# Performance work log

Hardware: AMD Instinct MI355X
Metric: run time of the kernel (lower is better)

The kernel has to match this reference:

```python
import jax, jax.numpy as jnp
import numpy as np

NH, HD = 12, 64          # heads, head dim (d_model=768)
SC = HD ** -0.5          # both Attention and CA_Attention use head_dim**-0.5


def patchify(x, p1, p2):
    # 'b c (h p1) (w p2) -> b (h w) (p1 p2 c)'
    B, C, H, W = x.shape
    h, w = H // p1, W // p2
    x = x.reshape(B, C, h, p1, w, p2).transpose(0, 2, 4, 3, 5, 1)  # b h w p1 p2 c
    return x.reshape(B, h * w, p1 * p2 * C)


def unpatchify(x, h, w, p1, p2, c):
    # 'b (h w) (p1 p2 c) -> b c (h p1) (w p2)'
    B = x.shape[0]
    x = x.reshape(B, h, w, p1, p2, c).transpose(0, 5, 1, 3, 2, 4)
    return x.reshape(B, c, h * p1, w * p2)


def ln(x, g, b):
    m = x.mean(-1, keepdims=True)
    v = ((x - m) ** 2).mean(-1, keepdims=True)
    return (x - m) / jnp.sqrt(v + 1e-5) * g + b


def setup_inputs() -> dict:
    key = jax.random.key(0)
    specs = [
        ('img_feats', (2, 32, 112, 112, 80)), ('txt', (2, 77, 768)),
        ('pe_w_ax', (1120, 768)), ('pe_b_ax', (768,)),
        ('pe_w_sag', (1120, 768)), ('pe_b_sag', (768,)),
        ('pe_w_cor', (1568, 768)), ('pe_b_cor', (768,)),
        ('pos_ax', (1, 256, 768)), ('pos_sag', (1, 256, 768)), ('pos_cor', (1, 256, 768)),
        ('qw', (768, 768)), ('kw', (768, 768)), ('vw', (768, 768)),
        ('pw', (768, 768)), ('pb', (768,)),
        ('caq_w', (768, 768)), ('caq_b', (768,)), ('cak_w', (768, 768)), ('cak_b', (768,)),
        ('cav_w', (768, 768)), ('cav_b', (768,)), ('cao_w', (768, 768)), ('cao_b', (768,)),
        ('mlp_w1', (768, 3072)), ('mlp_b1', (3072,)), ('mlp_w2', (3072, 768)), ('mlp_b2', (768,)),
        ('ow_ax', (768, 1120)), ('ob_ax', (1120,)),
        ('ow_sag', (768, 1120)), ('ob_sag', (1120,)),
        ('ow_cor', (768, 1568)), ('ob_cor', (1568,)),
    ]
    big = {'img_feats', 'txt', 'pos_ax', 'pos_sag', 'pos_cor'}
    out = {}
    for k, (n, s) in zip(jax.random.split(key, len(specs)), specs):
        scale = 1.0 if n in big else 0.02
        out[n] = jax.random.normal(k, s, jnp.float32) * scale
    out['view_w'] = jnp.ones((3,), jnp.float32)
    for n in ('n1_g', 'n2_g', 'n3_g'):
        out[n] = jnp.ones((768,), jnp.float32)
    for n in ('n1_b', 'n2_b', 'n3_b'):
        out[n] = jnp.zeros((768,), jnp.float32)
    return out


def reference(img_feats, txt, pe_w_ax, pe_b_ax, pe_w_sag, pe_b_sag, pe_w_cor, pe_b_cor,
              pos_ax, pos_sag, pos_cor, view_w, qw, kw, vw, pw, pb,
              caq_w, caq_b, cak_w, cak_b, cav_w, cav_b, cao_w, cao_b,
              n1_g, n1_b, n2_g, n2_b, n3_g, n3_b,
              mlp_w1, mlp_b1, mlp_w2, mlp_b2,
              ow_ax, ob_ax, ow_sag, ob_sag, ow_cor, ob_cor):

    def img_attn(t):
        B, N, C = t.shape
        q = (t @ qw).reshape(B, N, NH, HD)
        k = (t @ kw).reshape(B, N, NH, HD)
        v = (t @ vw).reshape(B, N, NH, HD)
        a = jax.nn.softmax(jnp.einsum('bnkc,bmkc->bknm', q, k) * SC, axis=-1)
        x = jnp.einsum('bknm,bmkc->bnkc', a, v).reshape(B, N, C)
        return x @ pw + pb

    def ca_attn(t, im):
        B, T, _ = t.shape
        N = im.shape[1]
        qh = (t @ caq_w + caq_b).reshape(B, T, NH, HD).transpose(0, 2, 1, 3)
        kh = (im @ cak_w + cak_b).reshape(B, N, NH, HD).transpose(0, 2, 1, 3)
        vh = (im @ cav_w + cav_b).reshape(B, N, NH, HD).transpose(0, 2, 1, 3)
        a = jax.nn.softmax(jnp.einsum('bhid,bhjd->bhij', qh, kh) * SC, axis=-1)
        # faithful to original einsum 'b h i j, b h j d -> b h j d' (sums over i)
        o = jnp.einsum('bhij,bhjd->bhjd', a, vh)
        o = o.transpose(0, 2, 1, 3).reshape(B, N, NH * HD)
        return o @ cao_w + cao_b

    def branch(v2d, pe_w, pe_b, pos, ow, ob, p1, p2):
        B, C, H, W = v2d.shape
        h, w = H // p1, W // p2
        q = patchify(v2d, p1, p2) @ pe_w + pe_b + pos
        q = ln(q, n1_g, n1_b)
        q = q + img_attn(q)
        q = ln(q, n2_g, n2_b)
        x = q + ca_attn(txt, q)
        x = x + (jax.nn.gelu(ln(x, n3_g, n3_b) @ mlp_w1 + mlp_b1, approximate=False) @ mlp_w2 + mlp_b2)
        return unpatchify(x @ ow + ob, h, w, p1, p2, C)

    # adaptive_avg_pool3d to size-1 along one axis == mean over that axis
    ax = img_feats.mean(2)    # (B,C,H,W)
    sag = img_feats.mean(3)   # (B,C,D,W)
    cor = img_feats.mean(4)   # (B,C,D,H)
    oax = branch(ax, pe_w_ax, pe_b_ax, pos_ax, ow_ax, ob_ax, 7, 5)
    osag = branch(sag, pe_w_sag, pe_b_sag, pos_sag, ow_sag, ob_sag, 7, 5)
    ocor = branch(cor, pe_w_cor, pe_b_cor, pos_cor, ow_cor, ob_cor, 7, 7)
    v3 = (view_w[0] * oax[:, :, None] + view_w[1] * osag[:, :, :, None]
          + view_w[2] * ocor[:, :, :, :, None])
    return img_feats + v3
```

## Files before the change

kernel.cpp:

```cpp
#include <hip/hip_runtime.h>
#include <math.h>

typedef __attribute__((ext_vector_type(8))) short s8;
typedef __attribute__((ext_vector_type(4))) float f4;
typedef unsigned short u16;

__device__ inline u16 f2bf(float f) {
    unsigned u = __float_as_uint(f);
    u += 0x7fffu + ((u >> 16) & 1u);
    return (u16)(u >> 16);
}
__device__ inline float bf2f(u16 x) {
    return __uint_as_float(((unsigned)x) << 16);
}
#define MFMA16(a, b, c) __builtin_amdgcn_mfma_f32_16x16x32_bf16(a, b, c, 0, 0, 0)

__global__ __launch_bounds__(256) void mean3_k(const float* __restrict__ img,
                                               float* __restrict__ axp,
                                               float* __restrict__ sag,
                                               float* __restrict__ cor) {
    __shared__ float sl[112*81];
    int blk = blockIdx.x;
    int dc = blk & 15, bc = blk >> 4;
    int d0 = dc * 7;
    int t = threadIdx.x;
    f4 axr[9];
    #pragma unroll
    for (int k = 0; k < 9; ++k) axr[k] = (f4){0.f,0.f,0.f,0.f};
    const float* base = img + (size_t)bc * 1003520 + (size_t)d0 * 8960;
    for (int sidx = 0; sidx < 7; ++sidx) {
        const f4* sp = reinterpret_cast<const f4*>(base + (size_t)sidx * 8960);
        #pragma unroll
        for (int k = 0; k < 9; ++k) {
            int q = t + k * 256;
            if (q < 2240) {
                f4 v = sp[q];
                axr[k] += v;
                int h = q / 20, w4 = q % 20;
                float* row = &sl[h * 81 + w4 * 4];
                row[0] = v[0]; row[1] = v[1]; row[2] = v[2]; row[3] = v[3];
            }
        }
        __syncthreads();
        if (t < 112) {
            float acc = 0.f;
            #pragma unroll 8
            for (int w = 0; w < 80; ++w) acc += sl[t * 81 + w];
            cor[((size_t)bc * 112 + d0 + sidx) * 112 + t] = acc * (1.f / 80.f);
        } else if (t < 192) {
            int w = t - 112;
            float acc = 0.f;
            #pragma unroll 8
            for (int h = 0; h < 112; ++h) acc += sl[h * 81 + w];
            sag[((size_t)bc * 112 + d0 + sidx) * 80 + w] = acc * (1.f / 112.f);
        }
        __syncthreads();
    }
    float* axo = axp + ((size_t)dc * 64 + bc) * 8960;
    #pragma unroll
    for (int k = 0; k < 9; ++k) {
        int q = t + k * 256;
        if (q < 2240) *reinterpret_cast<f4*>(axo + q * 4) = axr[k];
    }
}

struct TT {
    const float* in[16];
    u16* out[16];
    int K[16];
    int N[16];
    int start[16];
};

__global__ __launch_bounds__(256) void transp_all(TT tab) {
    __shared__ float tl[32][33];
    int bid = blockIdx.x;
    int e = 0;
    #pragma unroll
    for (int i = 1; i < 16; ++i) if (bid >= tab.start[i]) e = i;
    const float* in = tab.in[e];
    u16* out = tab.out[e];
    int K = tab.K[e], N = tab.N[e];
    int tid = bid - tab.start[e];
    int nt = N >> 5;
    int k0 = (tid / nt) * 32, n0 = (tid % nt) * 32;
    int t = threadIdx.x;
    int r = t >> 5, c = t & 31;
    #pragma unroll
    for (int i = 0; i < 4; ++i) tl[r + i*8][c] = in[(long)(k0 + r + i*8)*N + n0 + c];
    __syncthreads();
    #pragma unroll
    for (int i = 0; i < 4; ++i) out[(long)(n0 + r + i*8)*K + k0 + c] = f2bf(tl[c][r + i*8]);
}

__global__ __launch_bounds__(256) void patchify3_k(const float* __restrict__ axp,
                                                   const float* __restrict__ m_sag,
                                                   const float* __restrict__ m_cor,
                                                   u16* __restrict__ P0, u16* __restrict__ P1,
                                                   u16* __restrict__ P2) {
    __shared__ float sl[32][113];
    int br = blockIdx.y;
    int X = blockIdx.x;
    int b = X / 112, rem = X % 112;
    int hh = rem / 7, pp1 = rem % 7;
    const float* src; u16* dst; int Wt, p2, PD;
    if (br == 0)      { src = nullptr; dst = P0; Wt = 80;  p2 = 5; PD = 1120; }
    else if (br == 1) { src = m_sag;   dst = P1; Wt = 80;  p2 = 5; PD = 1120; }
    else              { src = m_cor;   dst = P2; Wt = 112; p2 = 7; PD = 1568; }
    int t = threadIdx.x;
    int row = hh*7 + pp1;
    int wq = Wt >> 2;
    if (br == 0) {
        for (int i = t; i < 32*20; i += 256) {
            int c = i / 20, w4 = i % 20;
            f4 s = (f4){0.f,0.f,0.f,0.f};
            size_t base = ((size_t)(b*32 + c)*112 + row)*80 + w4*4;
            #pragma unroll
            for (int p = 0; p < 16; ++p)
                s += *reinterpret_cast<const f4*>(axp + (size_t)p*573440 + base);
            s *= (1.f/112.f);
            sl[c][w4*4+0] = s[0]; sl[c][w4*4+1] = s[1]; sl[c][w4*4+2] = s[2]; sl[c][w4*4+3] = s[3];
        }
    } else {
        for (int i = t; i < 32*wq; i += 256) {
            int c = i / wq, w4 = i % wq;
            float4 v = *reinterpret_cast<const float4*>(
                src + ((size_t)(b*32 + c)*112 + row)*Wt + w4*4);
            sl[c][w4*4+0] = v.x; sl[c][w4*4+1] = v.y; sl[c][w4*4+2] = v.z; sl[c][w4*4+3] = v.w;
        }
    }
    __syncthreads();
    int tot = 16 * p2 * 32;
    for (int o = t; o < tot; o += 256) {
        int ww = o / (p2*32), rest = o % (p2*32);
        int pp2 = rest >> 5, c = rest & 31;
        dst[((size_t)(b*256 + hh*16 + ww))*PD + (pp1*p2 + pp2)*32 + c]
            = f2bf(sl[c][ww*p2 + pp2]);
    }
}

__device__ inline void load_tile(const u16* __restrict__ P, int ld, int nrows, int K,
                                 int r0, int k0, int t, s8 v[4]) {
    #pragma unroll
    for (int i = 0; i < 4; ++i) {
        int chunk = t + i*256;
        int row = chunk >> 4, c8 = (chunk & 15) * 8;
        s8 x;
        #pragma unroll
        for (int q = 0; q < 8; ++q) x[q] = 0;
        if (r0 + row < nrows && k0 + c8 < K)
            x = *reinterpret_cast<const s8*>(P + (long)(r0 + row)*ld + k0 + c8);
        v[i] = x;
    }
}
__device__ inline void load_tile_f32(const float* __restrict__ P, int ld, int nrows, int K,
                                     int r0, int k0, int t, s8 v[4]) {
    #pragma unroll
    for (int i = 0; i < 4; ++i) {
        int chunk = t + i*256;
        int row = chunk >> 4, c8 = (chunk & 15) * 8;
        s8 x;
        #pragma unroll
        for (int q = 0; q < 8; ++q) x[q] = 0;
        if (r0 + row < nrows && k0 + c8 < K) {
            const float* src = P + (long)(r0 + row)*ld + k0 + c8;
            #pragma unroll
            for (int q = 0; q < 8; ++q) x[q] = (short)f2bf(src[q]);
        }
        v[i] = x;
    }
}
__device__ inline void write_tile(u16 (*S)[136], int t, const s8 v[4]) {
    #pragma unroll
    for (int i = 0; i < 4; ++i) {
        int chunk = t + i*256;
        *reinterpret_cast<s8*>(&S[chunk >> 4][(chunk & 15)*8]) = v[i];
    }
}
__device__ inline void mfma_tile(const u16 (*As)[136], const u16 (*Bs)[136],
                                 int wr, int wc, int lane, f4 acc[2][2]) {
    int lrow = lane & 15;
    #pragma unroll
    for (int kh = 0; kh < 4; ++kh) {
        int lk = kh*32 + (lane >> 4) * 8;
        s8 af0 = *reinterpret_cast<const s8*>(&As[wr*32 + lrow][lk]);
        s8 af1 = *reinterpret_cast<const s8*>(&As[wr*32 + 16 + lrow][lk]);
        s8 bg0 = *reinterpret_cast<const s8*>(&Bs[wc*32 + lrow][lk]);
        s8 bg1 = *reinterpret_cast<const s8*>(&Bs[wc*32 + 16 + lrow][lk]);
        acc[0][0] = MFMA16(af0, bg0, acc[0][0]);
        acc[0][1] = MFMA16(af0, bg1, acc[0][1]);
        acc[1][0] = MFMA16(af1, bg0, acc[1][0]);
        acc[1][1] = MFMA16(af1, bg1, acc[1][1]);
    }
}

__global__ __launch_bounds__(256) void gemm_bf(
    const u16* __restrict__ A, const u16* __restrict__ Bt,
    float* __restrict__ Cf, u16* __restrict__ Cb,
    int M, int N, int K,
    const float* __restrict__ bias, const float* __restrict__ resid,
    int act)
{
    __shared__ u16 As[2][64][136];
    __shared__ u16 Bs[2][64][136];
    int t = threadIdx.x;
    int m0 = blockIdx.y * 64, n0 = blockIdx.x * 64;
    int wave = t >> 6, lane = t & 63;
    int wr = wave >> 1, wc = wave & 1;
    f4 acc[2][2];
    #pragma unroll
    for (int m = 0; m < 2; ++m)
        #pragma unroll
        for (int n = 0; n < 2; ++n)
            #pragma unroll
            for (int r = 0; r < 4; ++r) acc[m][n][r] = 0.f;
    int nk = (K + 127) >> 7;
    s8 pa[4], pbv[4];
    load_tile(A, K, M, K, m0, 0, t, pa);
    load_tile(Bt, K, N, K, n0, 0, t, pbv);
    write_tile(As[0], t, pa);
    write_tile(Bs[0], t, pbv);
    __syncthreads();
    for (int kt = 0; kt < nk; ++kt) {
        int cur = kt & 1;
        if (kt + 1 < nk) {
            load_tile(A, K, M, K, m0, (kt+1) << 7, t, pa);
            load_tile(Bt, K, N, K, n0, (kt+1) << 7, t, pbv);
        }
        mfma_tile(As[cur], Bs[cur], wr, wc, lane, acc);
        if (kt + 1 < nk) {
            write_tile(As[cur^1], t, pa);
            write_tile(Bs[cur^1], t, pbv);
        }
        __syncthreads();
    }
    #pragma unroll
    for (int m = 0; m < 2; ++m) {
        int rbase = m0 + wr*32 + m*16 + (lane >> 4) * 4;
        #pragma unroll
        for (int n = 0; n < 2; ++n) {
            int col = n0 + wc*32 + n*16 + (lane & 15);
            if (col >= N) continue;
            #pragma unroll
            for (int r = 0; r < 4; ++r) {
                int row = rbase + r;
                if (row >= M) continue;
                float v = acc[m][n][r];
                if (bias)  v += bias[col];
                if (resid) v += resid[(long)row * N + col];
                if (act == 1) v = 0.5f * v * (1.0f + erff(v * 0.70710678118654752f));
                long ci = (long)row * N + col;
                if (Cf) Cf[ci] = v;
                if (Cb) Cb[ci] = f2bf(v);
            }
        }
    }
}

__global__ __launch_bounds__(256) void gemm_big(
    const u16* __restrict__ A, const u16* __restrict__ Bt,
    u16* __restrict__ Cb, u16* __restrict__ vt,
    int N, int K,
    const float* __restrict__ bias, const float* __restrict__ bias2, int act)
{
    __shared__ u16 As[2][128][72];
    __shared__ u16 Bs[2][128][72];
    int t = threadIdx.x;
    int m0 = blockIdx.y * 128, n0 = blockIdx.x * 128;
    int wave = t >> 6, lane = t & 63;
    int wr = wave >> 1, wc = wave & 1;
    f4 acc[4][4];
    #pragma unroll
    for (int m = 0; m < 4; ++m)
        #pragma unroll
        for (int n = 0; n < 4; ++n)
            #pragma unroll
            for (int r = 0; r < 4; ++r) acc[m][n][r] = 0.f;
    int nk = K >> 6;
    s8 pa[4], pbv[4];
    #pragma unroll
    for (int i = 0; i < 4; ++i) {
        int chunk = t + i*256;
        pa[i]  = *reinterpret_cast<const s8*>(A  + (long)(m0 + (chunk>>3))*K + (chunk&7)*8);
        pbv[i] = *reinterpret_cast<const s8*>(Bt + (long)(n0 + (chunk>>3))*K + (chunk&7)*8);
    }
    #pragma unroll
    for (int i = 0; i < 4; ++i) {
        int chunk = t + i*256;
        *reinterpret_cast<s8*>(&As[0][chunk>>3][(chunk&7)*8]) = pa[i];
        *reinterpret_cast<s8*>(&Bs[0][chunk>>3][(chunk&7)*8]) = pbv[i];
    }
    __syncthreads();
    for (int kt = 0; kt < nk; ++kt) {
        int cur = kt & 1;
        if (kt + 1 < nk) {
            int k0 = (kt+1) << 6;
            #pragma unroll
            for (int i = 0; i < 4; ++i) {
                int chunk = t + i*256;
                pa[i]  = *reinterpret_cast<const s8*>(A  + (long)(m0 + (chunk>>3))*K + k0 + (chunk&7)*8);
                pbv[i] = *reinterpret_cast<const s8*>(Bt + (long)(n0 + (chunk>>3))*K + k0 + (chunk&7)*8);
            }
        }
        #pragma unroll
        for (int kh = 0; kh < 2; ++kh) {
            int lk = kh*32 + (lane >> 4) * 8;
            int lr = lane & 15;
            s8 af[4], bf[4];
            #pragma unroll
            for (int m = 0; m < 4; ++m)
                af[m] = *reinterpret_cast<const s8*>(&As[cur][wr*64 + m*16 + lr][lk]);
            #pragma unroll
            for (int n = 0; n < 4; ++n)
                bf[n] = *reinterpret_cast<const s8*>(&Bs[cur][wc*64 + n*16 + lr][lk]);
            #pragma unroll
            for (int m = 0; m < 4; ++m)
                #pragma unroll
                for (int n = 0; n < 4; ++n)
                    acc[m][n] = MFMA16(af[m], bf[n], acc[m][n]);
        }
        if (kt + 1 < nk) {
            #pragma unroll
            for (int i = 0; i < 4; ++i) {
                int chunk = t + i*256;
                *reinterpret_cast<s8*>(&As[cur^1][chunk>>3][(chunk&7)*8]) = pa[i];
                *reinterpret_cast<s8*>(&Bs[cur^1][chunk>>3][(chunk&7)*8]) = pbv[i];
            }
        }
        __syncthreads();
    }
    #pragma unroll
    for (int m = 0; m < 4; ++m) {
        int rbase = m0 + wr*64 + m*16 + (lane >> 4) * 4;
        #pragma unroll
        for (int n = 0; n < 4; ++n) {
            int col = n0 + wc*64 + n*16 + (lane & 15);
            #pragma unroll
            for (int r = 0; r < 4; ++r) {
                int row = rbase + r;
                float v = acc[m][n][r];
                if (bias) {
                    float bb = bias2 ? ((col < 768) ? bias[col] : bias2[col - 768]) : bias[col];
                    v += bb;
                }
                if (act == 1) v = 0.5f * v * (1.0f + erff(v * 0.70710678118654752f));
                u16 b = f2bf(v);
                Cb[(long)row * N + col] = b;
                if (vt && col >= 1536) {
                    int z = (row >> 8) * 12 + ((col - 1536) >> 6);
                    vt[((long)z * 64 + (col & 63)) * 256 + (row & 255)] = b;
                }
            }
        }
    }
}

struct PeDesc {
    const u16* A[3];
    const u16* Bt[4];
    const float* bias[4];
    const float* pos[3];
    int K[4];
    int M[4];
};

__global__ __launch_bounds__(256) void gemm_pe(PeDesc d, const float* __restrict__ txtf,
                                               float* __restrict__ C, u16* __restrict__ QHb) {
    int z = blockIdx.z;
    int M = d.M[z], K = d.K[z];
    int m0 = blockIdx.y * 64, n0 = blockIdx.x * 64;
    if (m0 >= M) return;
    __shared__ u16 As[2][64][136];
    __shared__ u16 Bs[2][64][136];
    const u16* Bb = d.Bt[z];
    const float* bias = d.bias[z];
    int t = threadIdx.x;
    int wave = t >> 6, lane = t & 63;
    int wr = wave >> 1, wc = wave & 1;
    f4 acc[2][2];
    #pragma unroll
    for (int m = 0; m < 2; ++m)
        #pragma unroll
        for (int n = 0; n < 2; ++n)
            #pragma unroll
            for (int r = 0; r < 4; ++r) acc[m][n][r] = 0.f;
    int nk = (K + 127) >> 7;
    s8 pa[4], pbv[4];
    if (z < 3) load_tile(d.A[z], K, M, K, m0, 0, t, pa);
    else       load_tile_f32(txtf, K, M, K, m0, 0, t, pa);
    load_tile(Bb, K, 768, K, n0, 0, t, pbv);
    write_tile(As[0], t, pa);
    write_tile(Bs[0], t, pbv);
    __syncthreads();
    for (int kt = 0; kt < nk; ++kt) {
        int cur = kt & 1;
        if (kt + 1 < nk) {
            if (z < 3) load_tile(d.A[z], K, M, K, m0, (kt+1) << 7, t, pa);
            else       load_tile_f32(txtf, K, M, K, m0, (kt+1) << 7, t, pa);
            load_tile(Bb, K, 768, K, n0, (kt+1) << 7, t, pbv);
        }
        mfma_tile(As[cur], Bs[cur], wr, wc, lane, acc);
        if (kt + 1 < nk) {
            write_tile(As[cur^1], t, pa);
            write_tile(Bs[cur^1], t, pbv);
        }
        __syncthreads();
    }
    #pragma unroll
    for (int m = 0; m < 2; ++m) {
        int rbase = m0 + wr*32 + m*16 + (lane >> 4) * 4;
        #pragma unroll
        for (int n = 0; n < 2; ++n) {
            int col = n0 + wc*32 + n*16 + (lane & 15);
            #pragma unroll
            for (int r = 0; r < 4; ++r) {
                int row = rbase + r;
                if (row >= M) continue;
                float v = acc[m][n][r] + bias[col];
                if (z < 3) {
                    v += d.pos[z][(long)(row & 255)*768 + col];
                    C[((long)z*512 + row) * 768 + col] = v;
                } else {
                    QHb[(long)row * 768 + col] = f2bf(v);
                }
            }
        }
    }
}

struct OwDesc {
    const u16* Bt[3];
    float* plane[3];
    const float* bias[3];
    int N[3];
    int p2[3];
    int Wd[3];
};

__global__ __launch_bounds__(256) void gemm_ow(OwDesc d, const u16* __restrict__ A,
                                               const float* __restrict__ vwp) {
    int z = blockIdx.z;
    int N = d.N[z];
    int n0 = blockIdx.x * 64;
    if (n0 >= N) return;
    __shared__ u16 As[2][64][136];
    __shared__ u16 Bs[2][64][136];
    const u16* Ab = A + (long)z * 512 * 768;
    const u16* Bb = d.Bt[z];
    int t = threadIdx.x;
    int m0 = blockIdx.y * 64;
    int wave = t >> 6, lane = t & 63;
    int wr = wave >> 1, wc = wave & 1;
    f4 acc[2][2];
    #pragma unroll
    for (int m = 0; m < 2; ++m)
        #pragma unroll
        for (int n = 0; n < 2; ++n)
            #pragma unroll
            for (int r = 0; r < 4; ++r) acc[m][n][r] = 0.f;
    s8 pa[4], pbv[4];
    load_tile(Ab, 768, 512, 768, m0, 0, t, pa);
    load_tile(Bb, 768, N, 768, n0, 0, t, pbv);
    write_tile(As[0], t, pa);
    write_tile(Bs[0], t, pbv);
    __syncthreads();
    for (int kt = 0; kt < 6; ++kt) {
        int cur = kt & 1;
        if (kt + 1 < 6) {
            load_tile(Ab, 768, 512, 768, m0, (kt+1) << 7, t, pa);
            load_tile(Bb, 768, N, 768, n0, (kt+1) << 7, t, pbv);
        }
        mfma_tile(As[cur], Bs[cur], wr, wc, lane, acc);
        if (kt + 1 < 6) {
            write_tile(As[cur^1], t, pa);
            write_tile(Bs[cur^1], t, pbv);
        }
        __syncthreads();
    }
    float* plane = d.plane[z];
    const float* bias = d.bias[z];
    int p2 = d.p2[z], Wd = d.Wd[z];
    float wt = vwp[z];
    #pragma unroll
    for (int m = 0; m < 2; ++m) {
        int rbase = m0 + wr*32 + m*16 + (lane >> 4) * 4;
        #pragma unroll
        for (int n = 0; n < 2; ++n) {
            int col = n0 + wc*32 + n*16 + (lane & 15);
            if (col >= N) continue;
            int pp = col >> 5, c = col & 31;
            int pp1 = pp / p2, pp2 = pp % p2;
            float bv = bias[col];
            #pragma unroll
            for (int r = 0; r < 4; ++r) {
                int row = rbase + r;
                int b = row >> 8, nn = row & 255;
                int hh = nn >> 4, ww = nn & 15;
                int ho = hh*7 + pp1, wo = ww*p2 + pp2;
                plane[((long)(b*32 + c)*112 + ho)*Wd + wo] = wt * (acc[m][n][r] + bv);
            }
        }
    }
}

__global__ __launch_bounds__(256) void ln_k(const float* __restrict__ in,
                                            float* __restrict__ outf,
                                            u16* __restrict__ outb,
                                            const float* __restrict__ g,
                                            const float* __restrict__ bta) {
    constexpr int N = 768;
    int row = blockIdx.x;
    const float* x = in + (size_t)row * N;
    int t = threadIdx.x;
    float v0 = x[t], v1 = x[t+256], v2 = x[t+512];
    float s = v0+v1+v2, s2 = v0*v0+v1*v1+v2*v2;
    #pragma unroll
    for (int off = 32; off > 0; off >>= 1) { s += __shfl_down(s, off); s2 += __shfl_down(s2, off); }
    __shared__ float red[8];
    int wid = t >> 6, lane = t & 63;
    if (lane == 0) { red[wid] = s; red[wid+4] = s2; }
    __syncthreads();
    if (t == 0) {
        float S = red[0]+red[1]+red[2]+red[3];
        float S2 = red[4]+red[5]+red[6]+red[7];
        float mean = S * (1.f/N);
        float var = S2 * (1.f/N) - mean*mean;
        red[0] = mean; red[1] = rsqrtf(var + 1e-5f);
    }
    __syncthreads();
    float mean = red[0], rstd = red[1];
    float y0 = (v0-mean)*rstd*g[t]     + bta[t];
    float y1 = (v1-mean)*rstd*g[t+256] + bta[t+256];
    float y2 = (v2-mean)*rstd*g[t+512] + bta[t+512];
    if (outf) {
        float* y = outf + (size_t)row * N;
        y[t] = y0; y[t+256] = y1; y[t+512] = y2;
    }
    if (outb) {
        u16* y = outb + (size_t)row * N;
        y[t] = f2bf(y0); y[t+256] = f2bf(y1); y[t+512] = f2bf(y2);
    }
}

__global__ __launch_bounds__(256) void attn_k(const u16* __restrict__ QKV,
                                              const u16* __restrict__ Vt,
                                              u16* __restrict__ O) {
    __shared__ u16 Ks[256][72];
    __shared__ u16 Ps[128][264];
    __shared__ u16 Vs[64][264];
    int zz = blockIdx.x;
    int bh = zz >> 1, half = zz & 1;
    int bb = bh / 12, h = bh % 12;
    long qrow0 = (long)bb*256 + half*128;
    int hcol = h*64;
    int t = threadIdx.x;
    int wave = t >> 6, lane = t & 63;
    int lr = lane & 15, lg = lane >> 4;
    #pragma unroll
    for (int i = 0; i < 8; ++i) {
        int chunk = t + i*256;
        int row = chunk >> 3, c8 = (chunk & 7)*8;
        *reinterpret_cast<s8*>(&Ks[row][c8]) =
            *reinterpret_cast<const s8*>(QKV + ((long)bb*256 + row)*2304 + 768 + hcol + c8);
    }
    #pragma unroll
    for (int i = 0; i < 8; ++i) {
        int chunk = t + i*256;
        int d = chunk >> 5, j8 = (chunk & 31)*8;
        *reinterpret_cast<s8*>(&Vs[d][j8]) =
            *reinterpret_cast<const s8*>(Vt + (long)bh*16384 + (long)d*256 + j8);
    }
    __syncthreads();
    f4 acc[2][16];
    #pragma unroll
    for (int m = 0; m < 2; ++m)
        #pragma unroll
        for (int n = 0; n < 16; ++n)
            #pragma unroll
            for (int r = 0; r < 4; ++r) acc[m][n][r] = 0.f;
    #pragma unroll
    for (int kh = 0; kh < 2; ++kh) {
        s8 af0 = *reinterpret_cast<const s8*>(QKV + (qrow0 + wave*32 + lr)*2304 + hcol + kh*32 + lg*8);
        s8 af1 = *reinterpret_cast<const s8*>(QKV + (qrow0 + wave*32 + 16 + lr)*2304 + hcol + kh*32 + lg*8);
        #pragma unroll
        for (int n = 0; n < 16; ++n) {
            s8 bf = *reinterpret_cast<const s8*>(&Ks[n*16 + lr][kh*32 + lg*8]);
            acc[0][n] = MFMA16(af0, bf, acc[0][n]);
            acc[1][n] = MFMA16(af1, bf, acc[1][n]);
        }
    }
    #pragma unroll
    for (int m = 0; m < 2; ++m)
        #pragma unroll
        for (int r = 0; r < 4; ++r) {
            float mx = -1e30f;
            #pragma unroll
            for (int n = 0; n < 16; ++n) mx = fmaxf(mx, acc[m][n][r]);
            #pragma unroll
            for (int o = 8; o; o >>= 1) mx = fmaxf(mx, __shfl_xor(mx, o));
            float l = 0.f;
            float p[16];
            #pragma unroll
            for (int n = 0; n < 16; ++n) {
                p[n] = __expf((acc[m][n][r] - mx) * 0.125f);
                l += p[n];
            }
            #pragma unroll
            for (int o = 8; o; o >>= 1) l += __shfl_xor(l, o);
            float inv = 1.f / l;
            int prow = wave*32 + m*16 + lg*4 + r;
            #pragma unroll
            for (int n = 0; n < 16; ++n)
                Ps[prow][n*16 + lr] = f2bf(p[n] * inv);
        }
    __syncthreads();
    f4 o2[2][4];
    #pragma unroll
    for (int m = 0; m < 2; ++m)
        #pragma unroll
        for (int n = 0; n < 4; ++n)
            #pragma unroll
            for (int r = 0; r < 4; ++r) o2[m][n][r] = 0.f;
    #pragma unroll
    for (int kh = 0; kh < 8; ++kh) {
        s8 pf0 = *reinterpret_cast<const s8*>(&Ps[wave*32 + lr][kh*32 + lg*8]);
        s8 pf1 = *reinterpret_cast<const s8*>(&Ps[wave*32 + 16 + lr][kh*32 + lg*8]);
        #pragma unroll
        for (int n = 0; n < 4; ++n) {
            s8 vf = *reinterpret_cast<const s8*>(&Vs[n*16 + lr][kh*32 + lg*8]);
            o2[0][n] = MFMA16(pf0, vf, o2[0][n]);
            o2[1][n] = MFMA16(pf1, vf, o2[1][n]);
        }
    }
    #pragma unroll
    for (int m = 0; m < 2; ++m)
        #pragma unroll
        for (int n = 0; n < 4; ++n)
            #pragma unroll
            for (int r = 0; r < 4; ++r)
                O[(qrow0 + wave*32 + m*16 + lg*4 + r)*768 + hcol + n*16 + lr] = f2bf(o2[m][n][r]);
}

__global__ __launch_bounds__(256) void ca_fused(const u16* __restrict__ QHb,
                                                const u16* __restrict__ KVHb,
                                                u16* __restrict__ O) {
    __shared__ u16 QHs[80][72];
    __shared__ u16 KHs[256][72];
    __shared__ float rmax[80][4];
    __shared__ float rsum[80][4];
    __shared__ float Wj[256];
    int bh = blockIdx.x;
    int rowblk = bh / 12, h = bh % 12;
    int bsel = rowblk & 1;
    int t = threadIdx.x;
    int wave = t >> 6, lane = t & 63;
    int lr = lane & 15, lg = lane >> 4;
    #pragma unroll
    for (int i = 0; i < 3; ++i) {
        int chunk = t + i*256;
        if (chunk < 640) {
            int row = chunk >> 3, c8 = (chunk & 7)*8;
            s8 v;
            #pragma unroll
            for (int q = 0; q < 8; ++q) v[q] = 0;
            if (row < 77)
                v = *reinterpret_cast<const s8*>(QHb + ((long)(bsel*77 + row))*768 + h*64 + c8);
            *reinterpret_cast<s8*>(&QHs[row][c8]) = v;
        }
    }
    #pragma unroll
    for (int i = 0; i < 8; ++i) {
        int chunk = t + i*256;
        int row = chunk >> 3, c8 = (chunk & 7)*8;
        *reinterpret_cast<s8*>(&KHs[row][c8]) =
            *reinterpret_cast<const s8*>(KVHb + ((long)rowblk*256 + row)*1536 + h*64 + c8);
    }
    __syncthreads();
    f4 acc[5][4];
    #pragma unroll
    for (int m = 0; m < 5; ++m)
        #pragma unroll
        for (int n = 0; n < 4; ++n)
            #pragma unroll
            for (int r = 0; r < 4; ++r) acc[m][n][r] = 0.f;
    #pragma unroll
    for (int kh = 0; kh < 2; ++kh) {
        s8 af[5], bf[4];
        #pragma unroll
        for (int m = 0; m < 5; ++m)
            af[m] = *reinterpret_cast<const s8*>(&QHs[m*16 + lr][kh*32 + lg*8]);
        #pragma unroll
        for (int n = 0; n < 4; ++n)
            bf[n] = *reinterpret_cast<const s8*>(&KHs[wave*64 + n*16 + lr][kh*32 + lg*8]);
        #pragma unroll
        for (int m = 0; m < 5; ++m)
            #pragma unroll
            for (int n = 0; n < 4; ++n)
                acc[m][n] = MFMA16(af[m], bf[n], acc[m][n]);
    }
    #pragma unroll
    for (int m = 0; m < 5; ++m)
        #pragma unroll
        for (int r = 0; r < 4; ++r) {
            float mx = -1e30f;
            #pragma unroll
            for (int n = 0; n < 4; ++n) mx = fmaxf(mx, acc[m][n][r]);
            #pragma unroll
            for (int o = 8; o; o >>= 1) mx = fmaxf(mx, __shfl_xor(mx, o));
            if (lr == 0) rmax[m*16 + lg*4 + r][wave] = mx;
        }
    __syncthreads();
    #pragma unroll
    for (int m = 0; m < 5; ++m)
        #pragma unroll
        for (int r = 0; r < 4; ++r) {
            int i = m*16 + lg*4 + r;
            float mi = fmaxf(fmaxf(rmax[i][0], rmax[i][1]), fmaxf(rmax[i][2], rmax[i][3]));
            float s = 0.f;
            #pragma unroll
            for (int n = 0; n < 4; ++n) s += __expf((acc[m][n][r] - mi) * 0.125f);
            #pragma unroll
            for (int o = 8; o; o >>= 1) s += __shfl_xor(s, o);
            if (lr == 0) rsum[i][wave] = s;
        }
    __syncthreads();
    float wn[4] = {0.f, 0.f, 0.f, 0.f};
    #pragma unroll
    for (int m = 0; m < 5; ++m)
        #pragma unroll
        for (int r = 0; r < 4; ++r) {
            int i = m*16 + lg*4 + r;
            if (i < 77) {
                float mi = fmaxf(fmaxf(rmax[i][0], rmax[i][1]), fmaxf(rmax[i][2], rmax[i][3]));
                float li = rsum[i][0] + rsum[i][1] + rsum[i][2] + rsum[i][3];
                float inv = 1.f / li;
                #pragma unroll
                for (int n = 0; n < 4; ++n)
                    wn[n] += __expf((acc[m][n][r] - mi) * 0.125f) * inv;
            }
        }
    #pragma unroll
    for (int n = 0; n < 4; ++n) {
        wn[n] += __shfl_xor(wn[n], 16);
        wn[n] += __shfl_xor(wn[n], 32);
    }
    if (lane < 16) {
        #pragma unroll
        for (int n = 0; n < 4; ++n) Wj[wave*64 + n*16 + lr] = wn[n];
    }
    __syncthreads();
    int d = t & 63;
    #pragma unroll 4
    for (int it = 0; it < 64; ++it) {
        int j = it*4 + (t >> 6);
        long row = (long)rowblk*256 + j;
        float vh = bf2f(KVHb[row*1536 + 768 + h*64 + d]);
        O[row*768 + h*64 + d] = f2bf(Wj[j] * vh);
    }
}

__global__ __launch_bounds__(256) void final_k(const float* __restrict__ img,
                                               const float* __restrict__ Aax,
                                               const float* __restrict__ Asag,
                                               const float* __restrict__ Acor,
                                               float* __restrict__ out) {
    int blk = blockIdx.x;
    int bc = blk / 112;
    const float4* ip = reinterpret_cast<const float4*>(img + (size_t)blk * 8960);
    const float4* ap = reinterpret_cast<const float4*>(Aax + (size_t)bc * 8960);
    const float4* sp = reinterpret_cast<const float4*>(Asag + (size_t)blk * 80);
    const float*  cp = Acor + (size_t)blk * 112;
    float4* op = reinterpret_cast<float4*>(out + (size_t)blk * 8960);
    int t = threadIdx.x;
    for (int q = t; q < 2240; q += 256) {
        int h = q / 20, w4 = q % 20;
        float4 iv = ip[q], av = ap[q], sv = sp[w4];
        float cv = cp[h];
        float4 o;
        o.x = iv.x + av.x + sv.x + cv;
        o.y = iv.y + av.y + sv.y + cv;
        o.z = iv.z + av.z + sv.z + cv;
        o.w = iv.w + av.w + sv.w + cv;
        op[q] = o;
    }
}

extern "C" void kernel_launch(void* const* d_in, const int* in_sizes, int n_in,
                              void* d_out, int out_size, void* d_ws, size_t ws_size,
                              hipStream_t stream) {
    (void)in_sizes; (void)n_in; (void)out_size; (void)ws_size;
    const float* img    = (const float*)d_in[0];
    const float* txt    = (const float*)d_in[1];
    const float* pe_w[3] = {(const float*)d_in[2], (const float*)d_in[4], (const float*)d_in[6]};
    const float* pe_b[3] = {(const float*)d_in[3], (const float*)d_in[5], (const float*)d_in[7]};
    const float* pos[3]  = {(const float*)d_in[8], (const float*)d_in[9], (const float*)d_in[10]};
    const float* qw = (const float*)d_in[11];
    const float* kw = (const float*)d_in[12];
    const float* vw_attn = (const float*)d_in[13];
    const float* pw = (const float*)d_in[14];
    const float* pb = (const float*)d_in[15];
    const float* caq_w = (const float*)d_in[16];
    const float* caq_b = (const float*)d_in[17];
    const float* cak_w = (const float*)d_in[18];
    const float* cak_b = (const float*)d_in[19];
    const float* cav_w = (const float*)d_in[20];
    const float* cav_b = (const float*)d_in[21];
    const float* cao_w = (const float*)d_in[22];
    const float* cao_b = (const float*)d_in[23];
    const float* mlp_w1 = (const float*)d_in[24];
    const float* mlp_b1 = (const float*)d_in[25];
    const float* mlp_w2 = (const float*)d_in[26];
    const float* mlp_b2 = (const float*)d_in[27];
    const float* ow[3] = {(const float*)d_in[28], (const float*)d_in[30], (const float*)d_in[32]};
    const float* ob[3] = {(const float*)d_in[29], (const float*)d_in[31], (const float*)d_in[33]};
    const float* view_w = (const float*)d_in[34];
    const float* n_g[3] = {(const float*)d_in[35], (const float*)d_in[36], (const float*)d_in[37]};
    const float* n_b[3] = {(const float*)d_in[38], (const float*)d_in[39], (const float*)d_in[40]};

    unsigned char* sb = (unsigned char*)d_out;
    size_t off = 0;
    auto B = [&](size_t bytes) -> void* {
        void* p = sb + off; off += (bytes + 511) & ~(size_t)511; return p;
    };
    u16* qkvT  = (u16*)B((size_t)2304*768*2);
    u16* pwT   = (u16*)B(768*768*2);
    u16* caqT  = (u16*)B(768*768*2);
    u16* cakvT = (u16*)B((size_t)1536*768*2);
    u16* caoT  = (u16*)B(768*768*2);
    u16* mlp1T = (u16*)B((size_t)3072*768*2);
    u16* mlp2T = (u16*)B((size_t)768*3072*2);
    u16* peT[3]; peT[0] = (u16*)B((size_t)768*1120*2); peT[1] = (u16*)B((size_t)768*1120*2); peT[2] = (u16*)B((size_t)768*1568*2);
    u16* owT[3]; owT[0] = (u16*)B((size_t)1120*768*2); owT[1] = (u16*)B((size_t)1120*768*2); owT[2] = (u16*)B((size_t)1568*768*2);
    float* axp   = (float*)B((size_t)16*573440*4);
    float* m_sag = (float*)B(573440*4);
    float* m_cor = (float*)B(802816*4);
    u16* P0 = (u16*)B((size_t)512*1120*2);
    u16* P1 = (u16*)B((size_t)512*1120*2);
    u16* P2 = (u16*)B((size_t)512*1568*2);
    float* X0  = (float*)B((size_t)1536*768*4);
    float* X1f = (float*)B((size_t)1536*768*4);
    float* X2  = (float*)B((size_t)1536*768*4);
    float* X3f = (float*)B((size_t)1536*768*4);
    float* X4  = (float*)B((size_t)1536*768*4);
    u16* X1b = (u16*)B((size_t)1536*768*2);
    u16* X3b = (u16*)B((size_t)1536*768*2);
    u16* X5b = (u16*)B((size_t)1536*768*2);
    u16* X6b = (u16*)B((size_t)1536*768*2);
    u16* QKVb = (u16*)B((size_t)1536*2304*2);
    u16* Obf = (u16*)B((size_t)1536*768*2);
    u16* Vt  = (u16*)B((size_t)72*64*256*2);
    u16* Hb  = (u16*)B((size_t)1536*3072*2);
    u16* KVHb = (u16*)B((size_t)1536*1536*2);
    u16* QHb  = (u16*)B((size_t)154*768*2);

    float* ws = (float*)d_ws;
    float* Aax  = ws;
    float* Asag = ws + 573440;
    float* Acor = ws + 1146880;

    TT tab;
    {
        const float* ins[16] = {qw, kw, vw_attn, pw, caq_w, cak_w, cav_w, cao_w,
                                mlp_w1, mlp_w2, pe_w[0], pe_w[1], pe_w[2], ow[0], ow[1], ow[2]};
        u16* outs[16] = {qkvT, qkvT + 768*768, qkvT + 2*768*768, pwT, caqT, cakvT,
                         cakvT + 768*768, caoT, mlp1T, mlp2T, peT[0], peT[1], peT[2],
                         owT[0], owT[1], owT[2]};
        int Ks[16] = {768,768,768,768,768,768,768,768, 768,3072, 1120,1120,1568, 768,768,768};
        int Ns[16] = {768,768,768,768,768,768,768,768, 3072,768, 768,768,768, 1120,1120,1568};
        int st = 0;
        for (int i = 0; i < 16; ++i) {
            tab.in[i] = ins[i]; tab.out[i] = outs[i]; tab.K[i] = Ks[i]; tab.N[i] = Ns[i];
            tab.start[i] = st;
            st += (Ks[i] >> 5) * (Ns[i] >> 5);
        }
        transp_all<<<st, 256, 0, stream>>>(tab);
    }

    mean3_k<<<1024, 256, 0, stream>>>(img, axp, m_sag, m_cor);
    patchify3_k<<<dim3(224,3), 256, 0, stream>>>(axp, m_sag, m_cor, P0, P1, P2);

    auto gemm = [&](const u16* A, const u16* Bt, float* Cf, u16* Cb,
                    int M, int N, int K, const float* bias, const float* resid, int act) {
        dim3 g((N+63)/64, (M+63)/64, 1);
        gemm_bf<<<g, 256, 0, stream>>>(A, Bt, Cf, Cb, M, N, K, bias, resid, act);
    };

    {
        PeDesc d;
        d.A[0] = P0; d.A[1] = P1; d.A[2] = P2;
        d.Bt[0] = peT[0]; d.Bt[1] = peT[1]; d.Bt[2] = peT[2]; d.Bt[3] = caqT;
        d.bias[0] = pe_b[0]; d.bias[1] = pe_b[1]; d.bias[2] = pe_b[2]; d.bias[3] = caq_b;
        d.pos[0] = pos[0]; d.pos[1] = pos[1]; d.pos[2] = pos[2];
        d.K[0] = 1120; d.K[1] = 1120; d.K[2] = 1568; d.K[3] = 768;
        d.M[0] = 512; d.M[1] = 512; d.M[2] = 512; d.M[3] = 154;
        gemm_pe<<<dim3(12,8,4), 256, 0, stream>>>(d, txt, X0, QHb);
    }

    ln_k<<<1536, 256, 0, stream>>>(X0, X1f, X1b, n_g[0], n_b[0]);
    gemm_big<<<dim3(18,12), 256, 0, stream>>>(X1b, qkvT, QKVb, Vt, 2304, 768, nullptr, nullptr, 0);
    attn_k<<<144, 256, 0, stream>>>(QKVb, Vt, Obf);
    gemm(Obf, pwT, X2, nullptr, 1536, 768, 768, pb, X1f, 0);
    ln_k<<<1536, 256, 0, stream>>>(X2, X3f, X3b, n_g[1], n_b[1]);
    gemm_big<<<dim3(12,12), 256, 0, stream>>>(X3b, cakvT, KVHb, nullptr, 1536, 768, cak_b, cav_b, 0);
    ca_fused<<<72, 256, 0, stream>>>(QHb, KVHb, Obf);
    gemm(Obf, caoT, X4, nullptr, 1536, 768, 768, cao_b, X3f, 0);
    ln_k<<<1536, 256, 0, stream>>>(X4, nullptr, X5b, n_g[2], n_b[2]);
    gemm_big<<<dim3(24,12), 256, 0, stream>>>(X5b, mlp1T, Hb, nullptr, 3072, 768, mlp_b1, nullptr, 1);
    gemm(Hb, mlp2T, nullptr, X6b, 1536, 768, 3072, mlp_b2, X4, 0);
    {
        OwDesc d;
        d.Bt[0] = owT[0]; d.Bt[1] = owT[1]; d.Bt[2] = owT[2];
        d.plane[0] = Aax; d.plane[1] = Asag; d.plane[2] = Acor;
        d.bias[0] = ob[0]; d.bias[1] = ob[1]; d.bias[2] = ob[2];
        d.N[0] = 1120; d.N[1] = 1120; d.N[2] = 1568;
        d.p2[0] = 5; d.p2[1] = 5; d.p2[2] = 7;
        d.Wd[0] = 80; d.Wd[1] = 80; d.Wd[2] = 112;
        gemm_ow<<<dim3(25,8,3), 256, 0, stream>>>(d, X6b, view_w);
    }

    final_k<<<7168, 256, 0, stream>>>(img, Aax, Asag, Acor, (float*)d_out);
}
```

Before: 445.9 us.

## Fuse trunk GEMM/LN/CA stages into two persistent cooperative kernels with grid sync

Replaces the chain of separate launches (PE GEMM, layernorms, QKV GEMM, projection GEMMs, cross-attention, MLP, output GEMM) with two persistent cooperative kernels. Each kernel loops over the stages using grid-stride tile loops, a shared-memory union, and grid-wide barriers between stages. This is meant to remove per-kernel launch and drain overhead between many small dependent kernels. In exchange, the grid is capped at the occupancy limit (at most 512 blocks), so some stages get less parallelism, and each grid sync adds its own cost.

New measurement: 885.1 us. 1.99x slower.

```diff
diff --git a/kernel.cpp b/kernel.cpp
--- a/kernel.cpp
+++ b/kernel.cpp
@@ -1,5 +1,8 @@
 #include <hip/hip_runtime.h>
+#include <hip/hip_cooperative_groups.h>
 #include <math.h>
+
+namespace cg = cooperative_groups;
 
 typedef __attribute__((ext_vector_type(8))) short s8;
 typedef __attribute__((ext_vector_type(4))) float f4;
@@ -14,6 +17,15 @@
     return __uint_as_float(((unsigned)x) << 16);
 }
 #define MFMA16(a, b, c) __builtin_amdgcn_mfma_f32_16x16x32_bf16(a, b, c, 0, 0, 0)
+
+struct SMemG64 { u16 As[2][64][136]; u16 Bs[2][64][136]; };
+struct SMemG128 { u16 As[2][128][72]; u16 Bs[2][128][72]; };
+struct SMemCA {
+    u16 QHs[80][72]; u16 KHs[256][72];
+    float rmax[80][4]; float rsum[80][4]; float Wj[256];
+};
+struct SMemLN { float red[8]; };
+union SMemU { SMemG64 g64; SMemG128 g128; SMemCA ca; SMemLN ln; };
 
 __global__ __launch_bounds__(256) void mean3_k(const float* __restrict__ img,
                                                float* __restrict__ axp,
@@ -194,20 +206,11 @@
     }
 }
 
-__global__ __launch_bounds__(256) void gemm_bf(
-    const u16* __restrict__ A, const u16* __restrict__ Bt,
-    float* __restrict__ Cf, u16* __restrict__ Cb,
-    int M, int N, int K,
-    const float* __restrict__ bias, const float* __restrict__ resid,
-    int act)
-{
-    __shared__ u16 As[2][64][136];
-    __shared__ u16 Bs[2][64][136];
-    int t = threadIdx.x;
-    int m0 = blockIdx.y * 64, n0 = blockIdx.x * 64;
+__device__ void g64_core(SMemG64& S, const u16* A, const float* Af32,
+                         const u16* Bt, int M, int N, int K,
+                         int m0, int n0, int t, f4 acc[2][2]) {
     int wave = t >> 6, lane = t & 63;
     int wr = wave >> 1, wc = wave & 1;
-    f4 acc[2][2];
     #pragma unroll
     for (int m = 0; m < 2; ++m)
         #pragma unroll
@@ -216,24 +219,33 @@
             for (int r = 0; r < 4; ++r) acc[m][n][r] = 0.f;
     int nk = (K + 127) >> 7;
     s8 pa[4], pbv[4];
-    load_tile(A, K, M, K, m0, 0, t, pa);
+    if (Af32) load_tile_f32(Af32, K, M, K, m0, 0, t, pa);
+    else      load_tile(A, K, M, K, m0, 0, t, pa);
     load_tile(Bt, K, N, K, n0, 0, t, pbv);
-    write_tile(As[0], t, pa);
-    write_tile(Bs[0], t, pbv);
+    write_tile(S.As[0], t, pa);
+    write_tile(S.Bs[0], t, pbv);
     __syncthreads();
     for (int kt = 0; kt < nk; ++kt) {
         int cur = kt & 1;
         if (kt + 1 < nk) {
-            load_tile(A, K, M, K, m0, (kt+1) << 7, t, pa);
+            if (Af32) load_tile_f32(Af32, K, M, K, m0, (kt+1) << 7, t, pa);
+            else      load_tile(A, K, M, K, m0, (kt+1) << 7, t, pa);
             load_tile(Bt, K, N, K, n0, (kt+1) << 7, t, pbv);
         }
-        mfma_tile(As[cur], Bs[cur], wr, wc, lane, acc);
+        mfma_tile(S.As[cur], S.Bs[cur], wr, wc, lane, acc);
         if (kt + 1 < nk) {
-            write_tile(As[cur^1], t, pa);
-            write_tile(Bs[cur^1], t, pbv);
+            write_tile(S.As[cur^1], t, pa);
+            write_tile(S.Bs[cur^1], t, pbv);
         }
         __syncthreads();
     }
+}
+
+__device__ void g64_epi_std(const f4 acc[2][2], int M, int N, int m0, int n0, int t,
+                            float* Cf, u16* Cb, const float* bias,
+                            const float* resid, int act) {
+    int wave = t >> 6, lane = t & 63;
+    int wr = wave >> 1, wc = wave & 1;
     #pragma unroll
     for (int m = 0; m < 2; ++m) {
         int rbase = m0 + wr*32 + m*16 + (lane >> 4) * 4;
@@ -257,288 +269,389 @@
     }
 }
 
-__global__ __launch_bounds__(256) void gemm_big(
-    const u16* __restrict__ A, const u16* __restrict__ Bt,
-    u16* __restrict__ Cb, u16* __restrict__ vt,
-    int N, int K,
-    const float* __restrict__ bias, const float* __restrict__ bias2, int act)
-{
-    __shared__ u16 As[2][128][72];
-    __shared__ u16 Bs[2][128][72];
-    int t = threadIdx.x;
-    int m0 = blockIdx.y * 128, n0 = blockIdx.x * 128;
-    int wave = t >> 6, lane = t & 63;
-    int wr = wave >> 1, wc = wave & 1;
-    f4 acc[4][4];
-    #pragma unroll
-    for (int m = 0; m < 4; ++m)
-        #pragma unroll
-        for (int n = 0; n < 4; ++n)
-            #pragma unroll
-            for (int r = 0; r < 4; ++r) acc[m][n][r] = 0.f;
-    int nk = K >> 6;
-    s8 pa[4], pbv[4];
-    #pragma unroll
-    for (int i = 0; i < 4; ++i) {
-        int chunk = t + i*256;
-        pa[i]  = *reinterpret_cast<const s8*>(A  + (long)(m0 + (chunk>>3))*K + (chunk&7)*8);
-        pbv[i] = *reinterpret_cast<const s8*>(Bt + (long)(n0 + (chunk>>3))*K + (chunk&7)*8);
-    }
-    #pragma unroll
-    for (int i = 0; i < 4; ++i) {
-        int chunk = t + i*256;
-        *reinterpret_cast<s8*>(&As[0][chunk>>3][(chunk&7)*8]) = pa[i];
-        *reinterpret_cast<s8*>(&Bs[0][chunk>>3][(chunk&7)*8]) = pbv[i];
-    }
-    __syncthreads();
-    for (int kt = 0; kt < nk; ++kt) {
-        int cur = kt & 1;
-        if (kt + 1 < nk) {
-            int k0 = (kt+1) << 6;
-            #pragma unroll
-            for (int i = 0; i < 4; ++i) {
-                int chunk = t + i*256;
-                pa[i]  = *reinterpret_cast<const s8*>(A  + (long)(m0 + (chunk>>3))*K + k0 + (chunk&7)*8);
-                pbv[i] = *reinterpret_cast<const s8*>(Bt + (long)(n0 + (chunk>>3))*K + k0 + (chunk&7)*8);
-            }
-        }
-        #pragma unroll
-        for (int kh = 0; kh < 2; ++kh) {
-            int lk = kh*32 + (lane >> 4) * 8;
-            int lr = lane & 15;
-            s8 af[4], bf[4];
-            #pragma unroll
-            for (int m = 0; m < 4; ++m)
-                af[m] = *reinterpret_cast<const s8*>(&As[cur][wr*64 + m*16 + lr][lk]);
-            #pragma unroll
-            for (int n = 0; n < 4; ++n)
-                bf[n] = *reinterpret_cast<const s8*>(&Bs[cur][wc*64 + n*16 + lr][lk]);
-            #pragma unroll
-            for (int m = 0; m < 4; ++m)
-                #pragma unroll
-                for (int n = 0; n < 4; ++n)
-                    acc[m][n] = MFMA16(af[m], bf[n], acc[m][n]);
-        }
-        if (kt + 1 < nk) {
-            #pragma unroll
-            for (int i = 0; i < 4; ++i) {
-                int chunk = t + i*256;
-                *reinterpret_cast<s8*>(&As[cur^1][chunk>>3][(chunk&7)*8]) = pa[i];
-                *reinterpret_cast<s8*>(&Bs[cur^1][chunk>>3][(chunk&7)*8]) = pbv[i];
-            }
-        }
-        __syncthreads();
-    }
-    #pragma unroll
-    for (int m = 0; m < 4; ++m) {
-        int rbase = m0 + wr*64 + m*16 + (lane >> 4) * 4;
-        #pragma unroll
-        for (int n = 0; n < 4; ++n) {
-            int col = n0 + wc*64 + n*16 + (lane & 15);
-            #pragma unroll
-            for (int r = 0; r < 4; ++r) {
-                int row = rbase + r;
-                float v = acc[m][n][r];
-                if (bias) {
-                    float bb = bias2 ? ((col < 768) ? bias[col] : bias2[col - 768]) : bias[col];
-                    v += bb;
-                }
-                if (act == 1) v = 0.5f * v * (1.0f + erff(v * 0.70710678118654752f));
-                u16 b = f2bf(v);
-                Cb[(long)row * N + col] = b;
-                if (vt && col >= 1536) {
-                    int z = (row >> 8) * 12 + ((col - 1536) >> 6);
-                    vt[((long)z * 64 + (col & 63)) * 256 + (row & 255)] = b;
-                }
-            }
-        }
-    }
-}
-
-struct PeDesc {
-    const u16* A[3];
-    const u16* Bt[4];
-    const float* bias[4];
-    const float* pos[3];
-    int K[4];
-    int M[4];
-};
-
-__global__ __launch_bounds__(256) void gemm_pe(PeDesc d, const float* __restrict__ txtf,
-                                               float* __restrict__ C, u16* __restrict__ QHb) {
-    int z = blockIdx.z;
-    int M = d.M[z], K = d.K[z];
-    int m0 = blockIdx.y * 64, n0 = blockIdx.x * 64;
-    if (m0 >= M) return;
-    __shared__ u16 As[2][64][136];
-    __shared__ u16 Bs[2][64][136];
-    const u16* Bb = d.Bt[z];
-    const float* bias = d.bias[z];
+__device__ void phase_g64(SMemU& sm, const u16* A, const u16* Bt,
+                          float* Cf, u16* Cb, int M, int N, int K,
+                          const float* bias, const float* resid, int act) {
+    int ntx = (N + 63) >> 6, nty = (M + 63) >> 6;
+    int ntiles = ntx * nty;
+    for (int tile = blockIdx.x; tile < ntiles; tile += gridDim.x) {
+        int m0 = (tile / ntx) * 64, n0 = (tile % ntx) * 64;
+        f4 acc[2][2];
+        g64_core(sm.g64, A, nullptr, Bt, M, N, K, m0, n0, threadIdx.x, acc);
+        g64_epi_std(acc, M, N, m0, n0, threadIdx.x, Cf, Cb, bias, resid, act);
+    }
+}
+
+__device__ void phase_g128(SMemU& sm, const u16* A, const u16* Bt,
+                           u16* Cb, u16* vt, int Mt, int Nt, int N, int K,
+                           const float* bias, const float* bias2, int act) {
+    SMemG128& S = sm.g128;
     int t = threadIdx.x;
     int wave = t >> 6, lane = t & 63;
     int wr = wave >> 1, wc = wave & 1;
-    f4 acc[2][2];
-    #pragma unroll
-    for (int m = 0; m < 2; ++m)
-        #pragma unroll
-        for (int n = 0; n < 2; ++n)
-            #pragma unroll
-            for (int r = 0; r < 4; ++r) acc[m][n][r] = 0.f;
-    int nk = (K + 127) >> 7;
-    s8 pa[4], pbv[4];
-    if (z < 3) load_tile(d.A[z], K, M, K, m0, 0, t, pa);
-    else       load_tile_f32(txtf, K, M, K, m0, 0, t, pa);
-    load_tile(Bb, K, 768, K, n0, 0, t, pbv);
-    write_tile(As[0], t, pa);
-    write_tile(Bs[0], t, pbv);
-    __syncthreads();
-    for (int kt = 0; kt < nk; ++kt) {
-        int cur = kt & 1;
-        if (kt + 1 < nk) {
-            if (z < 3) load_tile(d.A[z], K, M, K, m0, (kt+1) << 7, t, pa);
-            else       load_tile_f32(txtf, K, M, K, m0, (kt+1) << 7, t, pa);
-            load_tile(Bb, K, 768, K, n0, (kt+1) << 7, t, pbv);
-        }
-        mfma_tile(As[cur], Bs[cur], wr, wc, lane, acc);
-        if (kt + 1 < nk) {
-            write_tile(As[cur^1], t, pa);
-            write_tile(Bs[cur^1], t, pbv);
+    int ntiles = Mt * Nt;
+    for (int tile = blockIdx.x; tile < ntiles; tile += gridDim.x) {
+        int m0 = (tile / Nt) * 128, n0 = (tile % Nt) * 128;
+        f4 acc[4][4];
+        #pragma unroll
+        for (int m = 0; m < 4; ++m)
+            #pragma unroll
+            for (int n = 0; n < 4; ++n)
+                #pragma unroll
+                for (int r = 0; r < 4; ++r) acc[m][n][r] = 0.f;
+        int nk = K >> 6;
+        s8 pa[4], pbv[4];
+        #pragma unroll
+        for (int i = 0; i < 4; ++i) {
+            int chunk = t + i*256;
+            pa[i]  = *reinterpret_cast<const s8*>(A  + (long)(m0 + (chunk>>3))*K + (chunk&7)*8);
+            pbv[i] = *reinterpret_cast<const s8*>(Bt + (long)(n0 + (chunk>>3))*K + (chunk&7)*8);
+        }
+        #pragma unroll
+        for (int i = 0; i < 4; ++i) {
+            int chunk = t + i*256;
+            *reinterpret_cast<s8*>(&S.As[0][chunk>>3][(chunk&7)*8]) = pa[i];
+            *reinterpret_cast<s8*>(&S.Bs[0][chunk>>3][(chunk&7)*8]) = pbv[i];
         }
         __syncthreads();
-    }
-    #pragma unroll
-    for (int m = 0; m < 2; ++m) {
-        int rbase = m0 + wr*32 + m*16 + (lane >> 4) * 4;
-        #pragma unroll
-        for (int n = 0; n < 2; ++n) {
-            int col = n0 + wc*32 + n*16 + (lane & 15);
-            #pragma unroll
-            for (int r = 0; r < 4; ++r) {
-                int row = rbase + r;
-                if (row >= M) continue;
-                float v = acc[m][n][r] + bias[col];
-                if (z < 3) {
-                    v += d.pos[z][(long)(row & 255)*768 + col];
-                    C[((long)z*512 + row) * 768 + col] = v;
-                } else {
-                    QHb[(long)row * 768 + col] = f2bf(v);
+        for (int kt = 0; kt < nk; ++kt) {
+            int cur = kt & 1;
+            if (kt + 1 < nk) {
+                int k0 = (kt+1) << 6;
+                #pragma unroll
+                for (int i = 0; i < 4; ++i) {
+                    int chunk = t + i*256;
+                    pa[i]  = *reinterpret_cast<const s8*>(A  + (long)(m0 + (chunk>>3))*K + k0 + (chunk&7)*8);
+                    pbv[i] = *reinterpret_cast<const s8*>(Bt + (long)(n0 + (chunk>>3))*K + k0 + (chunk&7)*8);
                 }
             }
-        }
-    }
-}
-
-struct OwDesc {
-    const u16* Bt[3];
-    float* plane[3];
-    const float* bias[3];
-    int N[3];
-    int p2[3];
-    int Wd[3];
+            #pragma unroll
+            for (int kh = 0; kh < 2; ++kh) {
+                int lk = kh*32 + (lane >> 4) * 8;
+                int lr = lane & 15;
+                s8 af[4], bf[4];
+                #pragma unroll
+                for (int m = 0; m < 4; ++m)
+                    af[m] = *reinterpret_cast<const s8*>(&S.As[cur][wr*64 + m*16 + lr][lk]);
+                #pragma unroll
+                for (int n = 0; n < 4; ++n)
+                    bf[n] = *reinterpret_cast<const s8*>(&S.Bs[cur][wc*64 + n*16 + lr][lk]);
+                #pragma unroll
+                for (int m = 0; m < 4; ++m)
+                    #pragma unroll
+                    for (int n = 0; n < 4; ++n)
+                        acc[m][n] = MFMA16(af[m], bf[n], acc[m][n]);
+            }
+            if (kt + 1 < nk) {
+                #pragma unroll
+                for (int i = 0; i < 4; ++i) {
+                    int chunk = t + i*256;
+                    *reinterpret_cast<s8*>(&S.As[cur^1][chunk>>3][(chunk&7)*8]) = pa[i];
+                    *reinterpret_cast<s8*>(&S.Bs[cur^1][chunk>>3][(chunk&7)*8]) = pbv[i];
+                }
+            }
+            __syncthreads();
+        }
+        #pragma unroll
+        for (int m = 0; m < 4; ++m) {
+            int rbase = m0 + wr*64 + m*16 + (lane >> 4) * 4;
+            #pragma unroll
+            for (int n = 0; n < 4; ++n) {
+                int col = n0 + wc*64 + n*16 + (lane & 15);
+                #pragma unroll
+                for (int r = 0; r < 4; ++r) {
+                    int row = rbase + r;
+                    float v = acc[m][n][r];
+                    if (bias) {
+                        float bb = bias2 ? ((col < 768) ? bias[col] : bias2[col - 768]) : bias[col];
+                        v += bb;
+                    }
+                    if (act == 1) v = 0.5f * v * (1.0f + erff(v * 0.70710678118654752f));
+                    u16 b = f2bf(v);
+                    Cb[(long)row * N + col] = b;
+                    if (vt && col >= 1536) {
+                        int z = (row >> 8) * 12 + ((col - 1536) >> 6);
+                        vt[((long)z * 64 + (col & 63)) * 256 + (row & 255)] = b;
+                    }
+                }
+            }
+        }
+    }
+}
+
+__device__ void ln_rows(SMemLN& S, const float* in, float* outf, u16* outb,
+                        const float* g, const float* bta) {
+    int t = threadIdx.x;
+    int wid = t >> 6, lane = t & 63;
+    for (int row = blockIdx.x; row < 1536; row += gridDim.x) {
+        const float* x = in + (size_t)row * 768;
+        float v0 = x[t], v1 = x[t+256], v2 = x[t+512];
+        float s = v0+v1+v2, s2 = v0*v0+v1*v1+v2*v2;
+        #pragma unroll
+        for (int off = 32; off; off >>= 1) { s += __shfl_down(s, off); s2 += __shfl_down(s2, off); }
+        if (lane == 0) { S.red[wid] = s; S.red[wid+4] = s2; }
+        __syncthreads();
+        float mean = (S.red[0]+S.red[1]+S.red[2]+S.red[3]) * (1.f/768.f);
+        float var = (S.red[4]+S.red[5]+S.red[6]+S.red[7]) * (1.f/768.f) - mean*mean;
+        float rstd = rsqrtf(var + 1e-5f);
+        float y0 = (v0-mean)*rstd*g[t]     + bta[t];
+        float y1 = (v1-mean)*rstd*g[t+256] + bta[t+256];
+        float y2 = (v2-mean)*rstd*g[t+512] + bta[t+512];
+        if (outf) {
+            float* y = outf + (size_t)row * 768;
+            y[t] = y0; y[t+256] = y1; y[t+512] = y2;
+        }
+        if (outb) {
+            u16* y = outb + (size_t)row * 768;
+            y[t] = f2bf(y0); y[t+256] = f2bf(y1); y[t+512] = f2bf(y2);
+        }
+        __syncthreads();
+    }
+}
+
+__device__ void ca_phase(SMemU& sm, const u16* QHb, const u16* KVHb, u16* O) {
+    if (blockIdx.x >= 72) return;
+    SMemCA& C = sm.ca;
+    int bh = blockIdx.x;
+    int rowblk = bh / 12, h = bh % 12;
+    int bsel = rowblk & 1;
+    int t = threadIdx.x;
+    int wave = t >> 6, lane = t & 63;
+    int lr = lane & 15, lg = lane >> 4;
+    #pragma unroll
+    for (int i = 0; i < 3; ++i) {
+        int chunk = t + i*256;
+        if (chunk < 640) {
+            int row = chunk >> 3, c8 = (chunk & 7)*8;
+            s8 v;
+            #pragma unroll
+            for (int q = 0; q < 8; ++q) v[q] = 0;
+            if (row < 77)
+                v = *reinterpret_cast<const s8*>(QHb + ((long)(bsel*77 + row))*768 + h*64 + c8);
+            *reinterpret_cast<s8*>(&C.QHs[row][c8]) = v;
+        }
+    }
+    #pragma unroll
+    for (int i = 0; i < 8; ++i) {
+        int chunk = t + i*256;
+        int row = chunk >> 3, c8 = (chunk & 7)*8;
+        *reinterpret_cast<s8*>(&C.KHs[row][c8]) =
+            *reinterpret_cast<const s8*>(KVHb + ((long)rowblk*256 + row)*1536 + h*64 + c8);
+    }
+    __syncthreads();
+    f4 acc[5][4];
+    #pragma unroll
+    for (int m = 0; m < 5; ++m)
+        #pragma unroll
+        for (int n = 0; n < 4; ++n)
+            #pragma unroll
+            for (int r = 0; r < 4; ++r) acc[m][n][r] = 0.f;
+    #pragma unroll
+    for (int kh = 0; kh < 2; ++kh) {
+        s8 af[5], bf[4];
+        #pragma unroll
+        for (int m = 0; m < 5; ++m)
+            af[m] = *reinterpret_cast<const s8*>(&C.QHs[m*16 + lr][kh*32 + lg*8]);
+        #pragma unroll
+        for (int n = 0; n < 4; ++n)
+            bf[n] = *reinterpret_cast<const s8*>(&C.KHs[wave*64 + n*16 + lr][kh*32 + lg*8]);
+        #pragma unroll
+        for (int m = 0; m < 5; ++m)
+            #pragma unroll
+            for (int n = 0; n < 4; ++n)
+                acc[m][n] = MFMA16(af[m], bf[n], acc[m][n]);
+    }
+    #pragma unroll
+    for (int m = 0; m < 5; ++m)
+        #pragma unroll
+        for (int r = 0; r < 4; ++r) {
+            float mx = -1e30f;
+            #pragma unroll
+            for (int n = 0; n < 4; ++n) mx = fmaxf(mx, acc[m][n][r]);
+            #pragma unroll
+            for (int o = 8; o; o >>= 1) mx = fmaxf(mx, __shfl_xor(mx, o));
+            if (lr == 0) C.rmax[m*16 + lg*4 + r][wave] = mx;
+        }
+    __syncthreads();
+    #pragma unroll
+    for (int m = 0; m < 5; ++m)
+        #pragma unroll
+        for (int r = 0; r < 4; ++r) {
+            int i = m*16 + lg*4 + r;
+            float mi = fmaxf(fmaxf(C.rmax[i][0], C.rmax[i][1]), fmaxf(C.rmax[i][2], C.rmax[i][3]));
+            float s = 0.f;
+            #pragma unroll
+            for (int n = 0; n < 4; ++n) s += __expf((acc[m][n][r] - mi) * 0.125f);
+            #pragma unroll
+            for (int o = 8; o; o >>= 1) s += __shfl_xor(s, o);
+            if (lr == 0) C.rsum[i][wave] = s;
+        }
+    __syncthreads();
+    float wn[4] = {0.f, 0.f, 0.f, 0.f};
+    #pragma unroll
+    for (int m = 0; m < 5; ++m)
+        #pragma unroll
+        for (int r = 0; r < 4; ++r) {
+            int i = m*16 + lg*4 + r;
+            if (i < 77) {
+                float mi = fmaxf(fmaxf(C.rmax[i][0], C.rmax[i][1]), fmaxf(C.rmax[i][2], C.rmax[i][3]));
+                float li = C.rsum[i][0] + C.rsum[i][1] + C.rsum[i][2] + C.rsum[i][3];
+                float inv = 1.f / li;
+                #pragma unroll
+                for (int n = 0; n < 4; ++n)
+                    wn[n] += __expf((acc[m][n][r] - mi) * 0.125f) * inv;
+            }
+        }
+    #pragma unroll
+    for (int n = 0; n < 4; ++n) {
+        wn[n] += __shfl_xor(wn[n], 16);
+        wn[n] += __shfl_xor(wn[n], 32);
+    }
+    if (lane < 16) {
+        #pragma unroll
+        for (int n = 0; n < 4; ++n) C.Wj[wave*64 + n*16 + lr] = wn[n];
+    }
+    __syncthreads();
+    int d = t & 63;
+    #pragma unroll 4
+    for (int it = 0; it < 64; ++it) {
+        int j = it*4 + (t >> 6);
+        long row = (long)rowblk*256 + j;
+        float vh = bf2f(KVHb[row*1536 + 768 + h*64 + d]);
+        O[row*768 + h*64 + d] = f2bf(C.Wj[j] * vh);
+    }
+}
+
+struct T1Args {
+    const u16* P[3];
+    const u16* peT[3]; const u16* caqT;
+    const float* peb[3]; const float* caqb;
+    const float* pos[3];
+    const float* txt;
+    float* X0; u16* QHb;
+    const float* g0; const float* b0;
+    float* X1f; u16* X1b;
+    const u16* qkvT; u16* QKVb; u16* Vt;
+    int K[4];
 };
 
-__global__ __launch_bounds__(256) void gemm_ow(OwDesc d, const u16* __restrict__ A,
-                                               const float* __restrict__ vwp) {
-    int z = blockIdx.z;
-    int N = d.N[z];
-    int n0 = blockIdx.x * 64;
-    if (n0 >= N) return;
-    __shared__ u16 As[2][64][136];
-    __shared__ u16 Bs[2][64][136];
-    const u16* Ab = A + (long)z * 512 * 768;
-    const u16* Bb = d.Bt[z];
+__global__ __launch_bounds__(256, 2) void trunk1_k(T1Args a) {
+    __shared__ SMemU sm;
+    cg::grid_group grid = cg::this_grid();
     int t = threadIdx.x;
-    int m0 = blockIdx.y * 64;
-    int wave = t >> 6, lane = t & 63;
-    int wr = wave >> 1, wc = wave & 1;
-    f4 acc[2][2];
-    #pragma unroll
-    for (int m = 0; m < 2; ++m)
-        #pragma unroll
-        for (int n = 0; n < 2; ++n)
-            #pragma unroll
-            for (int r = 0; r < 4; ++r) acc[m][n][r] = 0.f;
-    s8 pa[4], pbv[4];
-    load_tile(Ab, 768, 512, 768, m0, 0, t, pa);
-    load_tile(Bb, 768, N, 768, n0, 0, t, pbv);
-    write_tile(As[0], t, pa);
-    write_tile(Bs[0], t, pbv);
-    __syncthreads();
-    for (int kt = 0; kt < 6; ++kt) {
-        int cur = kt & 1;
-        if (kt + 1 < 6) {
-            load_tile(Ab, 768, 512, 768, m0, (kt+1) << 7, t, pa);
-            load_tile(Bb, 768, N, 768, n0, (kt+1) << 7, t, pbv);
-        }
-        mfma_tile(As[cur], Bs[cur], wr, wc, lane, acc);
-        if (kt + 1 < 6) {
-            write_tile(As[cur^1], t, pa);
-            write_tile(Bs[cur^1], t, pbv);
-        }
-        __syncthreads();
-    }
-    float* plane = d.plane[z];
-    const float* bias = d.bias[z];
-    int p2 = d.p2[z], Wd = d.Wd[z];
-    float wt = vwp[z];
-    #pragma unroll
-    for (int m = 0; m < 2; ++m) {
-        int rbase = m0 + wr*32 + m*16 + (lane >> 4) * 4;
-        #pragma unroll
-        for (int n = 0; n < 2; ++n) {
-            int col = n0 + wc*32 + n*16 + (lane & 15);
-            if (col >= N) continue;
-            int pp = col >> 5, c = col & 31;
-            int pp1 = pp / p2, pp2 = pp % p2;
-            float bv = bias[col];
-            #pragma unroll
-            for (int r = 0; r < 4; ++r) {
-                int row = rbase + r;
-                int b = row >> 8, nn = row & 255;
-                int hh = nn >> 4, ww = nn & 15;
-                int ho = hh*7 + pp1, wo = ww*p2 + pp2;
-                plane[((long)(b*32 + c)*112 + ho)*Wd + wo] = wt * (acc[m][n][r] + bv);
+    for (int tile = blockIdx.x; tile < 324; tile += gridDim.x) {
+        int z, ty, tx;
+        if (tile < 288) { z = tile / 96; int r = tile % 96; ty = r / 12; tx = r % 12; }
+        else            { z = 3; int r = tile - 288; ty = r / 12; tx = r % 12; }
+        int M = (z < 3) ? 512 : 154;
+        int K = a.K[z];
+        f4 acc[2][2];
+        g64_core(sm.g64, (z < 3) ? a.P[z] : nullptr, (z == 3) ? a.txt : nullptr,
+                 (z < 3) ? a.peT[z] : a.caqT, M, 768, K, ty*64, tx*64, t, acc);
+        int wave = t >> 6, lane = t & 63;
+        int wr = wave >> 1, wc = wave & 1;
+        const float* bias = (z < 3) ? a.peb[z] : a.caqb;
+        #pragma unroll
+        for (int m = 0; m < 2; ++m) {
+            int rbase = ty*64 + wr*32 + m*16 + (lane >> 4) * 4;
+            #pragma unroll
+            for (int n = 0; n < 2; ++n) {
+                int col = tx*64 + wc*32 + n*16 + (lane & 15);
+                #pragma unroll
+                for (int r = 0; r < 4; ++r) {
+                    int row = rbase + r;
+                    if (row >= M) continue;
+                    float v = acc[m][n][r] + bias[col];
+                    if (z < 3) {
+                        v += a.pos[z][(long)(row & 255)*768 + col];
+                        a.X0[((long)z*512 + row) * 768 + col] = v;
+                    } else {
+                        a.QHb[(long)row * 768 + col] = f2bf(v);
+                    }
+                }
             }
         }
     }
-}
-
-__global__ __launch_bounds__(256) void ln_k(const float* __restrict__ in,
-                                            float* __restrict__ outf,
-                                            u16* __restrict__ outb,
-                                            const float* __restrict__ g,
-                                            const float* __restrict__ bta) {
-    constexpr int N = 768;
-    int row = blockIdx.x;
-    const float* x = in + (size_t)row * N;
+    grid.sync();
+    ln_rows(sm.ln, a.X0, a.X1f, a.X1b, a.g0, a.b0);
+    grid.sync();
+    phase_g128(sm, a.X1b, a.qkvT, a.QKVb, a.Vt, 12, 18, 2304, 768, nullptr, nullptr, 0);
+}
+
+struct T2Args {
+    const u16* Obf; const u16* pwT; const float* pb; const float* X1f; float* X2;
+    const float* g1; const float* b1; float* X3f; u16* X3b;
+    const u16* cakvT; const float* cakb; const float* cavb; u16* KVHb;
+    const u16* QHb; u16* Oca;
+    const u16* caoT; const float* caob; float* X4;
+    const float* g2; const float* b2; u16* X5b;
+    const u16* mlp1T; const float* mb1; u16* Hb;
+    const u16* mlp2T; const float* mb2; u16* X6b;
+    const u16* owT[3]; const float* ob[3];
+    float* plane[3]; const float* vw;
+};
+
+__global__ __launch_bounds__(256, 2) void trunk2_k(T2Args a) {
+    __shared__ SMemU sm;
+    cg::grid_group grid = cg::this_grid();
     int t = threadIdx.x;
-    float v0 = x[t], v1 = x[t+256], v2 = x[t+512];
-    float s = v0+v1+v2, s2 = v0*v0+v1*v1+v2*v2;
-    #pragma unroll
-    for (int off = 32; off > 0; off >>= 1) { s += __shfl_down(s, off); s2 += __shfl_down(s2, off); }
-    __shared__ float red[8];
-    int wid = t >> 6, lane = t & 63;
-    if (lane == 0) { red[wid] = s; red[wid+4] = s2; }
-    __syncthreads();
-    if (t == 0) {
-        float S = red[0]+red[1]+red[2]+red[3];
-        float S2 = red[4]+red[5]+red[6]+red[7];
-        float mean = S * (1.f/N);
-        float var = S2 * (1.f/N) - mean*mean;
-        red[0] = mean; red[1] = rsqrtf(var + 1e-5f);
-    }
-    __syncthreads();
-    float mean = red[0], rstd = red[1];
-    float y0 = (v0-mean)*rstd*g[t]     + bta[t];
-    float y1 = (v1-mean)*rstd*g[t+256] + bta[t+256];
-    float y2 = (v2-mean)*rstd*g[t+512] + bta[t+512];
-    if (outf) {
-        float* y = outf + (size_t)row * N;
-        y[t] = y0; y[t+256] = y1; y[t+512] = y2;
-    }
-    if (outb) {
-        u16* y = outb + (size_t)row * N;
-        y[t] = f2bf(y0); y[t+256] = f2bf(y1); y[t+512] = f2bf(y2);
+    phase_g64(sm, a.Obf, a.pwT, a.X2, nullptr, 1536, 768, 768, a.pb, a.X1f, 0);
+    grid.sync();
+    ln_rows(sm.ln, a.X2, a.X3f, a.X3b, a.g1, a.b1);
+    grid.sync();
+    phase_g128(sm, a.X3b, a.cakvT, a.KVHb, nullptr, 12, 12, 1536, 768, a.cakb, a.cavb, 0);
+    grid.sync();
+    ca_phase(sm, a.QHb, a.KVHb, a.Oca);
+    grid.sync();
+    phase_g64(sm, a.Oca, a.caoT, a.X4, nullptr, 1536, 768, 768, a.caob, a.X3f, 0);
+    grid.sync();
+    ln_rows(sm.ln, a.X4, nullptr, a.X5b, a.g2, a.b2);
+    grid.sync();
+    phase_g128(sm, a.X5b, a.mlp1T, a.Hb, nullptr, 12, 24, 3072, 768, a.mb1, nullptr, 1);
+    grid.sync();
+    phase_g64(sm, a.Hb, a.mlp2T, nullptr, a.X6b, 1536, 768, 3072, a.mb2, a.X4, 0);
+    grid.sync();
+    {
+        const int Nz[3] = {1120, 1120, 1568};
+        const int ntxz[3] = {18, 18, 25};
+        const int p2z[3] = {5, 5, 7};
+        const int Wdz[3] = {80, 80, 112};
+        for (int tile = blockIdx.x; tile < 488; tile += gridDim.x) {
+            int z, ty, tx;
+            if (tile < 144)      { z = 0; ty = tile / 18; tx = tile % 18; }
+            else if (tile < 288) { z = 1; int r = tile - 144; ty = r / 18; tx = r % 18; }
+            else                 { z = 2; int r = tile - 288; ty = r / 25; tx = r % 25; }
+            int N = Nz[z];
+            f4 acc[2][2];
+            g64_core(sm.g64, a.X6b + (long)z*512*768, nullptr, a.owT[z],
+                     512, N, 768, ty*64, tx*64, t, acc);
+            int wave = t >> 6, lane = t & 63;
+            int wr = wave >> 1, wc = wave & 1;
+            float* plane = a.plane[z];
+            const float* bias = a.ob[z];
+            int p2 = p2z[z], Wd = Wdz[z];
+            float wt = a.vw[z];
+            #pragma unroll
+            for (int m = 0; m < 2; ++m) {
+                int rbase = ty*64 + wr*32 + m*16 + (lane >> 4) * 4;
+                #pragma unroll
+                for (int n = 0; n < 2; ++n) {
+                    int col = tx*64 + wc*32 + n*16 + (lane & 15);
+                    if (col >= N) continue;
+                    int pp = col >> 5, c = col & 31;
+                    int pp1 = pp / p2, pp2 = pp % p2;
+                    float bv = bias[col];
+                    #pragma unroll
+                    for (int r = 0; r < 4; ++r) {
+                        int row = rbase + r;
+                        int b = row >> 8, nn = row & 255;
+                        int hh = nn >> 4, ww = nn & 15;
+                        plane[((long)(b*32 + c)*112 + hh*7 + pp1)*Wd + ww*p2 + pp2]
+                            = wt * (acc[m][n][r] + bv);
+                    }
+                }
+            }
+        }
     }
 }
 
@@ -639,124 +752,6 @@
             #pragma unroll
             for (int r = 0; r < 4; ++r)
                 O[(qrow0 + wave*32 + m*16 + lg*4 + r)*768 + hcol + n*16 + lr] = f2bf(o2[m][n][r]);
-}
-
-__global__ __launch_bounds__(256) void ca_fused(const u16* __restrict__ QHb,
-                                                const u16* __restrict__ KVHb,
-                                                u16* __restrict__ O) {
-    __shared__ u16 QHs[80][72];
-    __shared__ u16 KHs[256][72];
-    __shared__ float rmax[80][4];
-    __shared__ float rsum[80][4];
-    __shared__ float Wj[256];
-    int bh = blockIdx.x;
-    int rowblk = bh / 12, h = bh % 12;
-    int bsel = rowblk & 1;
-    int t = threadIdx.x;
-    int wave = t >> 6, lane = t & 63;
-    int lr = lane & 15, lg = lane >> 4;
-    #pragma unroll
-    for (int i = 0; i < 3; ++i) {
-        int chunk = t + i*256;
-        if (chunk < 640) {
-            int row = chunk >> 3, c8 = (chunk & 7)*8;
-            s8 v;
-            #pragma unroll
-            for (int q = 0; q < 8; ++q) v[q] = 0;
-            if (row < 77)
-                v = *reinterpret_cast<const s8*>(QHb + ((long)(bsel*77 + row))*768 + h*64 + c8);
-            *reinterpret_cast<s8*>(&QHs[row][c8]) = v;
-        }
-    }
-    #pragma unroll
-    for (int i = 0; i < 8; ++i) {
-        int chunk = t + i*256;
-        int row = chunk >> 3, c8 = (chunk & 7)*8;
-        *reinterpret_cast<s8*>(&KHs[row][c8]) =
-            *reinterpret_cast<const s8*>(KVHb + ((long)rowblk*256 + row)*1536 + h*64 + c8);
-    }
-    __syncthreads();
-    f4 acc[5][4];
-    #pragma unroll
-    for (int m = 0; m < 5; ++m)
-        #pragma unroll
-        for (int n = 0; n < 4; ++n)
-            #pragma unroll
-            for (int r = 0; r < 4; ++r) acc[m][n][r] = 0.f;
-    #pragma unroll
-    for (int kh = 0; kh < 2; ++kh) {
-        s8 af[5], bf[4];
-        #pragma unroll
-        for (int m = 0; m < 5; ++m)
-            af[m] = *reinterpret_cast<const s8*>(&QHs[m*16 + lr][kh*32 + lg*8]);
-        #pragma unroll
-        for (int n = 0; n < 4; ++n)
-            bf[n] = *reinterpret_cast<const s8*>(&KHs[wave*64 + n*16 + lr][kh*32 + lg*8]);
-        #pragma unroll
-        for (int m = 0; m < 5; ++m)
-            #pragma unroll
-            for (int n = 0; n < 4; ++n)
-                acc[m][n] = MFMA16(af[m], bf[n], acc[m][n]);
-    }
-    #pragma unroll
-    for (int m = 0; m < 5; ++m)
-        #pragma unroll
-        for (int r = 0; r < 4; ++r) {
-            float mx = -1e30f;
-            #pragma unroll
-            for (int n = 0; n < 4; ++n) mx = fmaxf(mx, acc[m][n][r]);
-            #pragma unroll
-            for (int o = 8; o; o >>= 1) mx = fmaxf(mx, __shfl_xor(mx, o));
-            if (lr == 0) rmax[m*16 + lg*4 + r][wave] = mx;
-        }
-    __syncthreads();
-    #pragma unroll
-    for (int m = 0; m < 5; ++m)
-        #pragma unroll
-        for (int r = 0; r < 4; ++r) {
-            int i = m*16 + lg*4 + r;
-            float mi = fmaxf(fmaxf(rmax[i][0], rmax[i][1]), fmaxf(rmax[i][2], rmax[i][3]));
-            float s = 0.f;
-            #pragma unroll
-            for (int n = 0; n < 4; ++n) s += __expf((acc[m][n][r] - mi) * 0.125f);
-            #pragma unroll
-            for (int o = 8; o; o >>= 1) s += __shfl_xor(s, o);
-            if (lr == 0) rsum[i][wave] = s;
-        }
-    __syncthreads();
-    float wn[4] = {0.f, 0.f, 0.f, 0.f};
-    #pragma unroll
-    for (int m = 0; m < 5; ++m)
-        #pragma unroll
-        for (int r = 0; r < 4; ++r) {
-            int i = m*16 + lg*4 + r;
-            if (i < 77) {
-                float mi = fmaxf(fmaxf(rmax[i][0], rmax[i][1]), fmaxf(rmax[i][2], rmax[i][3]));
-                float li = rsum[i][0] + rsum[i][1] + rsum[i][2] + rsum[i][3];
-                float inv = 1.f / li;
-                #pragma unroll
-                for (int n = 0; n < 4; ++n)
-                    wn[n] += __expf((acc[m][n][r] - mi) * 0.125f) * inv;
-            }
-        }
-    #pragma unroll
-    for (int n = 0; n < 4; ++n) {
-        wn[n] += __shfl_xor(wn[n], 16);
-        wn[n] += __shfl_xor(wn[n], 32);
-    }
-    if (lane < 16) {
-        #pragma unroll
-        for (int n = 0; n < 4; ++n) Wj[wave*64 + n*16 + lr] = wn[n];
-    }
-    __syncthreads();
-    int d = t & 63;
-    #pragma unroll 4
-    for (int it = 0; it < 64; ++it) {
-        int j = it*4 + (t >> 6);
-        long row = (long)rowblk*256 + j;
-        float vh = bf2f(KVHb[row*1536 + 768 + h*64 + d]);
-        O[row*768 + h*64 + d] = f2bf(Wj[j] * vh);
-    }
 }
 
 __global__ __launch_bounds__(256) void final_k(const float* __restrict__ img,
@@ -817,41 +812,42 @@
     const float* n_g[3] = {(const float*)d_in[35], (const float*)d_in[36], (const float*)d_in[37]};
     const float* n_b[3] = {(const float*)d_in[38], (const float*)d_in[39], (const float*)d_in[40]};
 
+    typedef unsigned short u16t;
     unsigned char* sb = (unsigned char*)d_out;
     size_t off = 0;
     auto B = [&](size_t bytes) -> void* {
         void* p = sb + off; off += (bytes + 511) & ~(size_t)511; return p;
     };
-    u16* qkvT  = (u16*)B((size_t)2304*768*2);
-    u16* pwT   = (u16*)B(768*768*2);
-    u16* caqT  = (u16*)B(768*768*2);
-    u16* cakvT = (u16*)B((size_t)1536*768*2);
-    u16* caoT  = (u16*)B(768*768*2);
-    u16* mlp1T = (u16*)B((size_t)3072*768*2);
-    u16* mlp2T = (u16*)B((size_t)768*3072*2);
-    u16* peT[3]; peT[0] = (u16*)B((size_t)768*1120*2); peT[1] = (u16*)B((size_t)768*1120*2); peT[2] = (u16*)B((size_t)768*1568*2);
-    u16* owT[3]; owT[0] = (u16*)B((size_t)1120*768*2); owT[1] = (u16*)B((size_t)1120*768*2); owT[2] = (u16*)B((size_t)1568*768*2);
+    u16t* qkvT  = (u16t*)B((size_t)2304*768*2);
+    u16t* pwT   = (u16t*)B(768*768*2);
+    u16t* caqT  = (u16t*)B(768*768*2);
+    u16t* cakvT = (u16t*)B((size_t)1536*768*2);
+    u16t* caoT  = (u16t*)B(768*768*2);
+    u16t* mlp1T = (u16t*)B((size_t)3072*768*2);
+    u16t* mlp2T = (u16t*)B((size_t)768*3072*2);
+    u16t* peT[3]; peT[0] = (u16t*)B((size_t)768*1120*2); peT[1] = (u16t*)B((size_t)768*1120*2); peT[2] = (u16t*)B((size_t)768*1568*2);
+    u16t* owT[3]; owT[0] = (u16t*)B((size_t)1120*768*2); owT[1] = (u16t*)B((size_t)1120*768*2); owT[2] = (u16t*)B((size_t)1568*768*2);
     float* axp   = (float*)B((size_t)16*573440*4);
     float* m_sag = (float*)B(573440*4);
     float* m_cor = (float*)B(802816*4);
-    u16* P0 = (u16*)B((size_t)512*1120*2);
-    u16* P1 = (u16*)B((size_t)512*1120*2);
-    u16* P2 = (u16*)B((size_t)512*1568*2);
+    u16t* P0 = (u16t*)B((size_t)512*1120*2);
+    u16t* P1 = (u16t*)B((size_t)512*1120*2);
+    u16t* P2 = (u16t*)B((size_t)512*1568*2);
     float* X0  = (float*)B((size_t)1536*768*4);
     float* X1f = (float*)B((size_t)1536*768*4);
     float* X2  = (float*)B((size_t)1536*768*4);
     float* X3f = (float*)B((size_t)1536*768*4);
     float* X4  = (float*)B((size_t)1536*768*4);
-    u16* X1b = (u16*)B((size_t)1536*768*2);
-    u16* X3b = (u16*)B((size_t)1536*768*2);
-    u16* X5b = (u16*)B((size_t)1536*768*2);
-    u16* X6b = (u16*)B((size_t)1536*768*2);
-    u16* QKVb = (u16*)B((size_t)1536*2304*2);
-    u16* Obf = (u16*)B((size_t)1536*768*2);
-    u16* Vt  = (u16*)B((size_t)72*64*256*2);
-    u16* Hb  = (u16*)B((size_t)1536*3072*2);
-    u16* KVHb = (u16*)B((size_t)1536*1536*2);
-    u16* QHb  = (u16*)B((size_t)154*768*2);
+    u16t* X1b = (u16t*)B((size_t)1536*768*2);
+    u16t* X3b = (u16t*)B((size_t)1536*768*2);
+    u16t* X5b = (u16t*)B((size_t)1536*768*2);
+    u16t* X6b = (u16t*)B((size_t)1536*768*2);
+    u16t* QKVb = (u16t*)B((size_t)1536*2304*2);
+    u16t* Obf = (u16t*)B((size_t)1536*768*2);
+    u16t* Vt  = (u16t*)B((size_t)72*64*256*2);
+    u16t* Hb  = (u16t*)B((size_t)1536*3072*2);
+    u16t* KVHb = (u16t*)B((size_t)1536*1536*2);
+    u16t* QHb  = (u16t*)B((size_t)154*768*2);
 
     float* ws = (float*)d_ws;
     float* Aax  = ws;
@@ -862,9 +858,9 @@
     {
         const float* ins[16] = {qw, kw, vw_attn, pw, caq_w, cak_w, cav_w, cao_w,
                                 mlp_w1, mlp_w2, pe_w[0], pe_w[1], pe_w[2], ow[0], ow[1], ow[2]};
-        u16* outs[16] = {qkvT, qkvT + 768*768, qkvT + 2*768*768, pwT, caqT, cakvT,
-                         cakvT + 768*768, caoT, mlp1T, mlp2T, peT[0], peT[1], peT[2],
-                         owT[0], owT[1], owT[2]};
+        u16t* outs[16] = {qkvT, qkvT + 768*768, qkvT + 2*768*768, pwT, caqT, cakvT,
+                          cakvT + 768*768, caoT, mlp1T, mlp2T, peT[0], peT[1], peT[2],
+                          owT[0], owT[1], owT[2]};
         int Ks[16] = {768,768,768,768,768,768,768,768, 768,3072, 1120,1120,1568, 768,768,768};
         int Ns[16] = {768,768,768,768,768,768,768,768, 3072,768, 768,768,768, 1120,1120,1568};
         int st = 0;
@@ -879,43 +875,48 @@
     mean3_k<<<1024, 256, 0, stream>>>(img, axp, m_sag, m_cor);
     patchify3_k<<<dim3(224,3), 256, 0, stream>>>(axp, m_sag, m_cor, P0, P1, P2);
 
-    auto gemm = [&](const u16* A, const u16* Bt, float* Cf, u16* Cb,
-                    int M, int N, int K, const float* bias, const float* resid, int act) {
-        dim3 g((N+63)/64, (M+63)/64, 1);
-        gemm_bf<<<g, 256, 0, stream>>>(A, Bt, Cf, Cb, M, N, K, bias, resid, act);
-    };
-
     {
-        PeDesc d;
-        d.A[0] = P0; d.A[1] = P1; d.A[2] = P2;
-        d.Bt[0] = peT[0]; d.Bt[1] = peT[1]; d.Bt[2] = peT[2]; d.Bt[3] = caqT;
-        d.bias[0] = pe_b[0]; d.bias[1] = pe_b[1]; d.bias[2] = pe_b[2]; d.bias[3] = caq_b;
-        d.pos[0] = pos[0]; d.pos[1] = pos[1]; d.pos[2] = pos[2];
-        d.K[0] = 1120; d.K[1] = 1120; d.K[2] = 1568; d.K[3] = 768;
-        d.M[0] = 512; d.M[1] = 512; d.M[2] = 512; d.M[3] = 154;
-        gemm_pe<<<dim3(12,8,4), 256, 0, stream>>>(d, txt, X0, QHb);
-    }
-
-    ln_k<<<1536, 256, 0, stream>>>(X0, X1f, X1b, n_g[0], n_b[0]);
-    gemm_big<<<dim3(18,12), 256, 0, stream>>>(X1b, qkvT, QKVb, Vt, 2304, 768, nullptr, nullptr, 0);
+        int occ = 0;
+        hipOccupancyMaxActiveBlocksPerMultiprocessor(&occ, trunk1_k, 256, 0);
+        if (occ < 1) occ = 1;
+        int g1 = occ * 256; if (g1 > 512) g1 = 512;
+        T1Args a;
+        a.P[0] = P0; a.P[1] = P1; a.P[2] = P2;
+        a.peT[0] = peT[0]; a.peT[1] = peT[1]; a.peT[2] = peT[2]; a.caqT = caqT;
+        a.peb[0] = pe_b[0]; a.peb[1] = pe_b[1]; a.peb[2] = pe_b[2]; a.caqb = caq_b;
+        a.pos[0] = pos[0]; a.pos[1] = pos[1]; a.pos[2] = pos[2];
+        a.txt = txt; a.X0 = X0; a.QHb = QHb;
+        a.g0 = n_g[0]; a.b0 = n_b[0]; a.X1f = X1f; a.X1b = X1b;
+        a.qkvT = qkvT; a.QKVb = QKVb; a.Vt = Vt;
+        a.K[0] = 1120; a.K[1] = 1120; a.K[2] = 1568; a.K[3] = 768;
+        void* args[] = { (void*)&a };
+        hipLaunchCooperativeKernel(reinterpret_cast<void*>(trunk1_k),
+                                   dim3(g1), dim3(256), args, 0, stream);
+    }
+
     attn_k<<<144, 256, 0, stream>>>(QKVb, Vt, Obf);
-    gemm(Obf, pwT, X2, nullptr, 1536, 768, 768, pb, X1f, 0);
-    ln_k<<<1536, 256, 0, stream>>>(X2, X3f, X3b, n_g[1], n_b[1]);
-    gemm_big<<<dim3(12,12), 256, 0, stream>>>(X3b, cakvT, KVHb, nullptr, 1536, 768, cak_b, cav_b, 0);
-    ca_fused<<<72, 256, 0, stream>>>(QHb, KVHb, Obf);
-    gemm(Obf, caoT, X4, nullptr, 1536, 768, 768, cao_b, X3f, 0);
-    ln_k<<<1536, 256, 0, stream>>>(X4, nullptr, X5b, n_g[2], n_b[2]);
-    gemm_big<<<dim3(24,12), 256, 0, stream>>>(X5b, mlp1T, Hb, nullptr, 3072, 768, mlp_b1, nullptr, 1);
-    gemm(Hb, mlp2T, nullptr, X6b, 1536, 768, 3072, mlp_b2, X4, 0);
+
     {
-        OwDesc d;
-        d.Bt[0] = owT[0]; d.Bt[1] = owT[1]; d.Bt[2] = owT[2];
-        d.plane[0] = Aax; d.plane[1] = Asag; d.plane[2] = Acor;
-        d.bias[0] = ob[0]; d.bias[1] = ob[1]; d.bias[2] = ob[2];
-        d.N[0] = 1120; d.N[1] = 1120; d.N[2] = 1568;
-        d.p2[0] = 5; d.p2[1] = 5; d.p2[2] = 7;
-        d.Wd[0] = 80; d.Wd[1] = 80; d.Wd[2] = 112;
-        gemm_ow<<<dim3(25,8,3), 256, 0, stream>>>(d, X6b, view_w);
+        int occ = 0;
+        hipOccupancyMaxActiveBlocksPerMultiprocessor(&occ, trunk2_k, 256, 0);
+        if (occ < 1) occ = 1;
+        int g2 = occ * 256; if (g2 > 512) g2 = 512;
+        T2Args a;
+        a.Obf = Obf; a.pwT = pwT; a.pb = pb; a.X1f = X1f; a.X2 = X2;
+        a.g1 = n_g[1]; a.b1 = n_b[1]; a.X3f = X3f; a.X3b = X3b;
+        a.cakvT = cakvT; a.cakb = cak_b; a.cavb = cav_b; a.KVHb = KVHb;
+        a.QHb = QHb; a.Oca = Obf;
+        a.caoT = caoT; a.caob = cao_b; a.X4 = X4;
+        a.g2 = n_g[2]; a.b2 = n_b[2]; a.X5b = X5b;
+        a.mlp1T = mlp1T; a.mb1 = mlp_b1; a.Hb = Hb;
+        a.mlp2T = mlp2T; a.mb2 = mlp_b2; a.X6b = X6b;
+        a.owT[0] = owT[0]; a.owT[1] = owT[1]; a.owT[2] = owT[2];
+        a.ob[0] = ob[0]; a.ob[1] = ob[1]; a.ob[2] = ob[2];
+        a.plane[0] = Aax; a.plane[1] = Asag; a.plane[2] = Acor;
+        a.vw = view_w;
+        void* args[] = { (void*)&a };
+        hipLaunchCooperativeKernel(reinterpret_cast<void*>(trunk2_k),
+                                   dim3(g2), dim3(256), args, 0, stream);
     }
 
     final_k<<<7168, 256, 0, stream>>>(img, Aax, Asag, Acor, (float*)d_out);
```
